# Performance work log

Measured on AMD Instinct MI355X. Metric: run time of the kernel, lower is better.

## Reference

```python
import jax, jax.numpy as jnp
import numpy as np

EPS = 1e-8
ITERS = 4
NEG = -1e9

def build_grid(H, W):
    y = jnp.linspace(-1.0, 1.0, H)
    x = jnp.linspace(-1.0, 1.0, W)
    yy, xx = jnp.meshgrid(y, x, indexing='ij')
    return jnp.stack([xx, yy], axis=-1)[None]  # (1,H,W,2)

def ln(x, g, b):
    m = jnp.mean(x, -1, keepdims=True)
    v = jnp.mean(jnp.square(x - m), -1, keepdims=True)
    return (x - m) * jax.lax.rsqrt(v + 1e-5) * g + b

def gru(x, h, wih, whh, bih, bhh):
    gi = x @ wih.T + bih
    gh = h @ whh.T + bhh
    ir, iz, inn = jnp.split(gi, 3, -1)
    hr, hz, hn = jnp.split(gh, 3, -1)
    r = jax.nn.sigmoid(ir + hr)
    z = jax.nn.sigmoid(iz + hz)
    n = jnp.tanh(inn + r * hn)
    return (1.0 - z) * n + z * h


def setup_inputs():
    B, H, W, C, D, K = 4, 128, 128, 64, 64, 4
    keys = iter(jax.random.split(jax.random.key(0), 64))
    def nrm(shape, s):
        return jax.random.normal(next(keys), shape, jnp.float32) * s
    sw = C ** -0.5
    sd = D ** -0.5
    inp = dict(
        feat=nrm((B, H, W, C), 1.0),
        mask=jax.random.randint(next(keys), (K, 1, H, W), 0, 2).astype(jnp.float32),
        noise_fg=nrm((B, K, D), 1.0),
        noise_bg=nrm((B, 1, D), 1.0),
        slots_mu=nrm((1, 1, D), 1.0),
        slots_logsigma=nrm((1, 1, D), 0.1),
        slots_mu_bg=nrm((1, 1, D), 1.0),
        slots_logsigma_bg=nrm((1, 1, D), 0.1),
        norm_feat_g=jnp.ones((C,)), norm_feat_b=jnp.zeros((C,)),
        grid_embed_w=nrm((C, 4), 0.5), grid_embed_b=jnp.zeros((C,)),
        k_fg_w=nrm((C, C), sw), v_fg_w=nrm((C, C), sw),
        k_bg_w=nrm((C, C), sw), v_bg_w=nrm((C, C), sw),
        mlp_fg_ln_g=jnp.ones((C,)), mlp_fg_ln_b=jnp.zeros((C,)),
        mlp_fg_w=nrm((D, C), sw), mlp_fg_b=jnp.zeros((D,)),
        mlp_bg_ln_g=jnp.ones((C,)), mlp_bg_ln_b=jnp.zeros((C,)),
        mlp_bg_w=nrm((D, C), sw), mlp_bg_b=jnp.zeros((D,)),
        q_ln_g=jnp.ones((D,)), q_ln_b=jnp.zeros((D,)), q_w=nrm((D, D), sd),
        qbg_ln_g=jnp.ones((D,)), qbg_ln_b=jnp.zeros((D,)), qbg_w=nrm((D, D), sd),
        gru_fg_wih=nrm((3 * D, D), sd), gru_fg_whh=nrm((3 * D, D), sd),
        gru_fg_bih=jnp.zeros((3 * D,)), gru_fg_bhh=jnp.zeros((3 * D,)),
        gru_bg_wih=nrm((3 * D, D), sd), gru_bg_whh=nrm((3 * D, D), sd),
        gru_bg_bih=jnp.zeros((3 * D,)), gru_bg_bhh=jnp.zeros((3 * D,)),
        res_fg_ln_g=jnp.ones((D,)), res_fg_ln_b=jnp.zeros((D,)),
        res_fg_w=nrm((D, D), sd), res_fg_b=jnp.zeros((D,)),
        res_bg_ln_g=jnp.ones((D,)), res_bg_ln_b=jnp.zeros((D,)),
        res_bg_w=nrm((D, D), sd), res_bg_b=jnp.zeros((D,)),
    )
    return inp


def reference(feat, mask, noise_fg, noise_bg, slots_mu, slots_logsigma,
              slots_mu_bg, slots_logsigma_bg, norm_feat_g, norm_feat_b,
              grid_embed_w, grid_embed_b, k_fg_w, v_fg_w, k_bg_w, v_bg_w,
              mlp_fg_ln_g, mlp_fg_ln_b, mlp_fg_w, mlp_fg_b,
              mlp_bg_ln_g, mlp_bg_ln_b, mlp_bg_w, mlp_bg_b,
              q_ln_g, q_ln_b, q_w, qbg_ln_g, qbg_ln_b, qbg_w,
              gru_fg_wih, gru_fg_whh, gru_fg_bih, gru_fg_bhh,
              gru_bg_wih, gru_bg_whh, gru_bg_bih, gru_bg_bhh,
              res_fg_ln_g, res_fg_ln_b, res_fg_w, res_fg_b,
              res_bg_ln_g, res_bg_ln_b, res_bg_w, res_bg_b):
    B, H, W, C = feat.shape
    N = H * W
    K = mask.shape[0]
    D = slots_mu.shape[-1]
    scale = D ** -0.5
    grid = build_grid(H, W)            # (1,H,W,2)
    grid_flat = grid.reshape(N, 2)
    feat = feat.reshape(B, N, C)
    # slot init (noise passed in for determinism)
    slot_fg = slots_mu + jnp.exp(slots_logsigma) * noise_fg       # (B,K,D)
    slot_bg = slots_mu_bg + jnp.exp(slots_logsigma_bg) * noise_bg  # (B,1,D)
    # fg positions = mask-weighted grid mean
    gk = jnp.transpose(grid[0], (2, 0, 1))[None]  # (1,2,H,W)
    fg_pos = (gk * mask).sum((2, 3)) / (mask.sum((1, 2, 3))[:, None] + 1e-5)  # (K,2)
    fg_pos = jnp.broadcast_to(fg_pos[None], (B, K, 2))
    feat = ln(feat, norm_feat_g, norm_feat_b)
    # background k,v (position-independent, computed once)
    rel_bg = jnp.concatenate([grid, -grid], -1).reshape(1, 1, N, 4)
    ge_bg = rel_bg @ grid_embed_w.T + grid_embed_b                # (1,1,N,C)
    kb = (feat @ k_bg_w.T)[:, None] + ge_bg                       # (B,1,N,C)
    vb = (feat @ v_bg_w.T)[:, None] + ge_bg
    k_bg = ln(kb, mlp_bg_ln_g, mlp_bg_ln_b) @ mlp_bg_w.T + mlp_bg_b
    v_bg = ln(vb, mlp_bg_ln_g, mlp_bg_ln_b) @ mlp_bg_w.T + mlp_bg_b
    mask_flat = mask.reshape(K, N)
    kf = feat @ k_fg_w.T   # iteration-invariant input projections
    vf = feat @ v_fg_w.T
    for _ in range(ITERS):
        prev_fg, prev_bg = slot_fg, slot_bg
        q_fg = ln(slot_fg, q_ln_g, q_ln_b) @ q_w.T
        q_bg = ln(slot_bg, qbg_ln_g, qbg_ln_b) @ qbg_w.T
        # position-relative grid embedding -> per-slot k,v
        rel = grid[:, None] - fg_pos[:, :, None, None, :]          # (B,K,H,W,2)
        rel = jnp.concatenate([rel, -rel], -1).reshape(B, K, N, 4)
        ge = rel @ grid_embed_w.T + grid_embed_b                   # (B,K,N,C)
        k = ln(kf[:, None] + ge, mlp_fg_ln_g, mlp_fg_ln_b) @ mlp_fg_w.T + mlp_fg_b
        v = ln(vf[:, None] + ge, mlp_fg_ln_g, mlp_fg_ln_b) @ mlp_fg_w.T + mlp_fg_b
        # background update
        attn_bg = jax.nn.softmax(jnp.einsum('bd,bnd->bn', q_bg[:, 0], k_bg[:, 0]) * scale, axis=1) + EPS
        upd_bg = jnp.einsum('bn,bnd->bd', attn_bg, v_bg[:, 0])
        sbg = gru(upd_bg, slot_bg[:, 0], gru_bg_wih, gru_bg_whh, gru_bg_bih, gru_bg_bhh)[:, None]
        slot_bg = ln(sbg, res_bg_ln_g, res_bg_ln_b) @ res_bg_w.T + res_bg_b + prev_bg
        # foreground update (vectorized over K slots)
        logits = jnp.einsum('bkd,bknd->bkn', q_fg, k) * scale
        logits = jnp.where(mask_flat[None] == 0, NEG, logits)
        attn = jax.nn.softmax(logits, axis=-1)
        upd_fg = jnp.einsum('bkn,bknd->bkd', attn, v)
        fg_pos = jnp.einsum('bkn,nd->bkd', attn, grid_flat)
        sfg = gru(upd_fg.reshape(-1, D), slot_fg.reshape(-1, D),
                  gru_fg_wih, gru_fg_whh, gru_fg_bih, gru_fg_bhh).reshape(B, K, D)
        slot_fg = ln(sfg, res_fg_ln_g, res_fg_ln_b) @ res_fg_w.T + res_fg_b + prev_fg
    slots = jnp.concatenate([slot_bg, slot_fg], axis=1)  # (B,K+1,D)
    return slots, fg_pos
```

## Files before the change

### kernel.cpp

```cpp
#include <hip/hip_runtime.h>
#include <math.h>

#define DEVI __device__ __forceinline__

constexpr int Bb = 4, Nn = 16384, Kk = 4;
constexpr int NCH = 64;
constexpr int CH = 256;
constexpr int FG_BLK = Bb * NCH;
constexpr int NBG = 64;
constexpr int BG_BLK = Bb * NBG;
constexpr int FG_PS = 72;
constexpr int BG_PS = 130;

typedef __attribute__((ext_vector_type(8))) short bf16x8;
typedef __attribute__((ext_vector_type(8))) unsigned short u16x8;
typedef __attribute__((ext_vector_type(4))) unsigned short u16x4;
typedef __attribute__((ext_vector_type(4))) float f32x4;

DEVI float bf2f(unsigned short u){ unsigned int x = ((unsigned int)u) << 16; return __builtin_bit_cast(float, x); }
DEVI unsigned short f2bf(float f){
  unsigned int u = __builtin_bit_cast(unsigned int, f);
  u += 0x7fffu + ((u >> 16) & 1u);
  return (unsigned short)(u >> 16);
}
DEVI float rsum_16_32(float v){ v += __shfl_xor(v,16); v += __shfl_xor(v,32); return v; }
DEVI float rmax_16_32(float v){ v = fmaxf(v,__shfl_xor(v,16)); v = fmaxf(v,__shfl_xor(v,32)); return v; }
DEVI float rsum_1_8(float v){ v += __shfl_xor(v,1); v += __shfl_xor(v,2); v += __shfl_xor(v,4); v += __shfl_xor(v,8); return v; }
DEVI float rmax_1_8(float v){ v = fmaxf(v,__shfl_xor(v,1)); v = fmaxf(v,__shfl_xor(v,2)); v = fmaxf(v,__shfl_xor(v,4)); v = fmaxf(v,__shfl_xor(v,8)); return v; }
DEVI float rsum_all(float v){ return rsum_16_32(rsum_1_8(v)); }
DEVI float rmax_all(float v){ return rmax_16_32(rmax_1_8(v)); }
DEVI float sel4(float a0, float a1, float a2, float a3, int r){
  float v = a0; v = (r == 1) ? a1 : v; v = (r == 2) ? a2 : v; v = (r == 3) ? a3 : v; return v;
}
DEVI float sigm(float x){ return 1.f / (1.f + __expf(-x)); }

constexpr float GSTEP = 2.0f / 127.0f;
DEVI float gxf(int n){ return (float)(n & 127) * GSTEP - 1.0f; }
DEVI float gyf(int n){ return (float)((n >> 7) & 127) * GSTEP - 1.0f; }

#define NEGINF (-__builtin_inff())

__global__ __launch_bounds__(1024) void k_setup(
    const float* __restrict__ mask,
    const float* __restrict__ gw, const float* __restrict__ gb,
    const float* __restrict__ g_fg, const float* __restrict__ bln_fg,
    const float* __restrict__ w_fg, const float* __restrict__ b_fg,
    float* __restrict__ fg_pos, float* __restrict__ cbuf)
{
  int t = threadIdx.x;
  if (blockIdx.x < 4) {
    int k = blockIdx.x;
    const float4* mp = (const float4*)(mask + (size_t)k * Nn);
    float sm = 0, sx = 0, sy = 0;
    #pragma unroll
    for (int i = 0; i < 4; ++i) {
      int idx = t + i * 1024;
      float4 v = mp[idx];
      int n = idx * 4;
      float gy = gyf(n);
      float rowsum = v.x + v.y + v.z + v.w;
      sm += rowsum;
      sx += v.x * gxf(n) + v.y * gxf(n + 1) + v.z * gxf(n + 2) + v.w * gxf(n + 3);
      sy += rowsum * gy;
    }
    sm = rsum_all(sm); sx = rsum_all(sx); sy = rsum_all(sy);
    __shared__ float red[3][16];
    int wv = t >> 6, l = t & 63;
    if (l == 0) { red[0][wv] = sm; red[1][wv] = sx; red[2][wv] = sy; }
    __syncthreads();
    if (t == 0) {
      float S = 0, X = 0, Y = 0;
      #pragma unroll
      for (int i = 0; i < 16; ++i) { S += red[0][i]; X += red[1][i]; Y += red[2][i]; }
      float inv = 1.f / (S + 1e-5f);
      float px = X * inv, py = Y * inv;
      for (int b = 0; b < 4; ++b) { fg_pos[(b*4+k)*2+0] = px; fg_pos[(b*4+k)*2+1] = py; }
    }
  } else {
    if (t < 64) {
      float gx_t = gw[t*4+0] - gw[t*4+2];
      float gy_t = gw[t*4+1] - gw[t*4+3];
      float aGx = 0, aGy = 0, agW = 0, aC0 = 0;
      for (int c = 0; c < 64; ++c) {
        float wv = w_fg[t*64 + c];
        float gc = g_fg[c];
        float gxc = gw[c*4+0] - gw[c*4+2];
        float gyc = gw[c*4+1] - gw[c*4+3];
        aGx += gxc * gc * wv;
        aGy += gyc * gc * wv;
        agW += gc * wv;
        aC0 += bln_fg[c] * wv;
      }
      cbuf[t] = aGx; cbuf[64+t] = aGy; cbuf[128+t] = agW; cbuf[192+t] = aC0 + b_fg[t];
      float mgx = rsum_all(gx_t) * (1.f/64.f);
      float mgy = rsum_all(gy_t) * (1.f/64.f);
      float egx2 = rsum_all(gx_t*gx_t) * (1.f/64.f);
      float egy2 = rsum_all(gy_t*gy_t) * (1.f/64.f);
      float egxy = rsum_all(gx_t*gy_t) * (1.f/64.f);
      if (t == 0) { cbuf[256]=mgx; cbuf[257]=mgy; cbuf[258]=egx2; cbuf[259]=egy2; cbuf[260]=egxy; }
    }
  }
}

__global__ __launch_bounds__(256) void k_prep(
    const float* __restrict__ feat,
    const float* __restrict__ norm_g, const float* __restrict__ norm_b,
    const float* __restrict__ gw, const float* __restrict__ gb,
    const float* __restrict__ k_fg_w, const float* __restrict__ v_fg_w,
    const float* __restrict__ k_bg_w, const float* __restrict__ v_bg_w,
    const float* __restrict__ mlp_bg_ln_g, const float* __restrict__ mlp_bg_ln_b,
    const float* __restrict__ mlp_bg_w, const float* __restrict__ mlp_bg_b,
    const float* __restrict__ mlp_fg_ln_g, const float* __restrict__ mlp_fg_w,
    unsigned short* __restrict__ A_k, unsigned short* __restrict__ A_vT,
    float* __restrict__ statsKV,
    unsigned short* __restrict__ kbg, unsigned short* __restrict__ vbg,
    const float* __restrict__ noise_fg, const float* __restrict__ noise_bg,
    const float* __restrict__ mu, const float* __restrict__ ls,
    const float* __restrict__ mub, const float* __restrict__ lsb,
    const float* __restrict__ q_ln_g, const float* __restrict__ q_ln_b, const float* __restrict__ q_w,
    const float* __restrict__ qbg_ln_g, const float* __restrict__ qbg_ln_b, const float* __restrict__ qbg_w,
    const float* __restrict__ cbuf,
    float* slot_fg, float* slot_bg, float* q_fg, float* q_bg, float* qscal)
{
  int tid = threadIdx.x, wave = tid >> 6, l = tid & 63;
  if ((int)blockIdx.x >= 512) {
    __shared__ float lds[64];
    int ib = blockIdx.x - 512;
    float lnv = 0.f;
    if (tid < 64) {
      if (ib < 16) {
        float s = mu[tid] + expf(ls[tid]) * noise_fg[ib * 64 + tid];
        slot_fg[ib * 64 + tid] = s;
        float mean = rsum_all(s) * (1.f / 64.f);
        float d = s - mean;
        float var = rsum_all(d * d) * (1.f / 64.f);
        lnv = d * rsqrtf(var + 1e-5f) * q_ln_g[tid] + q_ln_b[tid];
      } else {
        int b = ib - 16;
        float s = mub[tid] + expf(lsb[tid]) * noise_bg[b * 64 + tid];
        slot_bg[b * 64 + tid] = s;
        float mean = rsum_all(s) * (1.f / 64.f);
        float d = s - mean;
        float var = rsum_all(d * d) * (1.f / 64.f);
        lnv = d * rsqrtf(var + 1e-5f) * qbg_ln_g[tid] + qbg_ln_b[tid];
      }
      lds[tid] = lnv;
    }
    __syncthreads();
    if (tid < 64) {
      if (ib < 16) {
        float acc = 0.f;
        #pragma unroll 8
        for (int c = 0; c < 64; ++c) acc += q_w[tid * 64 + c] * lds[c];
        q_fg[ib * 64 + tid] = acc;
        float qGx = rsum_all(acc * cbuf[tid]);
        float qGy = rsum_all(acc * cbuf[64 + tid]);
        float qgW = rsum_all(acc * cbuf[128 + tid]);
        float qC0 = rsum_all(acc * cbuf[192 + tid]);
        if (tid == 0) { qscal[ib*4+0]=qGx; qscal[ib*4+1]=qGy; qscal[ib*4+2]=qgW; qscal[ib*4+3]=qC0; }
      } else {
        int b = ib - 16;
        float acc = 0.f;
        #pragma unroll 8
        for (int c = 0; c < 64; ++c) acc += qbg_w[tid * 64 + c] * lds[c];
        q_bg[b * 64 + tid] = acc;
      }
    }
    return;
  }
  __shared__ bf16x8 wfrag[6 * 8 * 64];
  __shared__ __align__(16) unsigned short tbuf[4][16][88];
  __shared__ float s_gwx[64], s_gwy[64], s_gb[64], s_mlg[64], s_mlb[64], s_mbb[64], s_gf[64];
  const float* wsrc[6] = { k_fg_w, v_fg_w, k_bg_w, v_bg_w, mlp_bg_w, mlp_fg_w };
  for (int mi = wave; mi < 6; mi += 4) {
    const float* ws = wsrc[mi];
    #pragma unroll
    for (int f = 0; f < 8; ++f) {
      int ct = f >> 1, kh = f & 1;
      int row = ct * 16 + (l & 15);
      int c0 = ((l >> 4) << 3) + kh * 32;
      bf16x8 v;
      #pragma unroll
      for (int j = 0; j < 8; ++j) v[j] = (short)f2bf(ws[row * 64 + c0 + j]);
      wfrag[(mi * 8 + f) * 64 + l] = v;
    }
  }
  if (tid < 64) {
    s_gwx[tid] = gw[tid*4+0] - gw[tid*4+2];
    s_gwy[tid] = gw[tid*4+1] - gw[tid*4+3];
    s_gb[tid]  = gb[tid];
    s_mlg[tid] = mlp_bg_ln_g[tid];
    s_mlb[tid] = mlp_bg_ln_b[tid];
    s_mbb[tid] = mlp_bg_b[tid];
    s_gf[tid]  = mlp_fg_ln_g[tid];
  }
  __syncthreads();

  int cb = (l >> 4) << 3;
  float ngr[16], nbr[16];
  #pragma unroll
  for (int j = 0; j < 16; ++j) {
    int col = (j < 8) ? (cb + j) : (32 + cb + j - 8);
    ngr[j] = norm_g[col]; nbr[j] = norm_b[col];
  }
  float gwxD[4], gwyD[4], gbD[4], mlgD[4], mlbD[4], mbbD[4], gfD[4];
  #pragma unroll
  for (int ct = 0; ct < 4; ++ct) {
    int col = ct * 16 + (l & 15);
    gwxD[ct] = s_gwx[col]; gwyD[ct] = s_gwy[col]; gbD[ct] = s_gb[col];
    mlgD[ct] = s_mlg[col]; mlbD[ct] = s_mlb[col]; mbbD[ct] = s_mbb[col];
    gfD[ct] = s_gf[col];
  }

  int wg = blockIdx.x * 4 + wave;
  for (int tt = 0; tt < 2; ++tt) {
    int tile = wg * 2 + tt;
    int rowg = tile * 16 + (l & 15);
    const float* fp = feat + (size_t)rowg * 64;
    float x[16];
    #pragma unroll
    for (int j = 0; j < 8; ++j) x[j] = fp[cb + j];
    #pragma unroll
    for (int j = 0; j < 8; ++j) x[8 + j] = fp[32 + cb + j];
    float sm = 0;
    #pragma unroll
    for (int j = 0; j < 16; ++j) sm += x[j];
    float mean = rsum_16_32(sm) * (1.f / 64.f);
    float vv = 0;
    #pragma unroll
    for (int j = 0; j < 16; ++j) { float d = x[j] - mean; vv += d * d; }
    float rstd = rsqrtf(rsum_16_32(vv) * (1.f / 64.f) + 1e-5f);
    bf16x8 a0, a1;
    #pragma unroll
    for (int j = 0; j < 8; ++j) a0[j] = (short)f2bf((x[j] - mean) * rstd * ngr[j] + nbr[j]);
    #pragma unroll
    for (int j = 0; j < 8; ++j) a1[j] = (short)f2bf((x[8 + j] - mean) * rstd * ngr[8 + j] + nbr[8 + j]);

    for (int mi = 0; mi < 4; ++mi) {
      f32x4 acc[4];
      #pragma unroll
      for (int ct = 0; ct < 4; ++ct) acc[ct] = (f32x4){0.f, 0.f, 0.f, 0.f};
      #pragma unroll
      for (int ct = 0; ct < 4; ++ct) {
        acc[ct] = __builtin_amdgcn_mfma_f32_16x16x32_bf16(a0, wfrag[(mi * 8 + ct * 2 + 0) * 64 + l], acc[ct], 0, 0, 0);
        acc[ct] = __builtin_amdgcn_mfma_f32_16x16x32_bf16(a1, wfrag[(mi * 8 + ct * 2 + 1) * 64 + l], acc[ct], 0, 0, 0);
      }
      if (mi < 2) {
        #pragma unroll
        for (int ct = 0; ct < 4; ++ct)
          #pragma unroll
          for (int r = 0; r < 4; ++r)
            acc[ct][r] += gbD[ct];
        float s1[4], s2[4], sx[4], sy[4];
        #pragma unroll
        for (int r = 0; r < 4; ++r) {
          float a0v = acc[0][r], a1v = acc[1][r], a2v = acc[2][r], a3v = acc[3][r];
          s1[r] = rsum_1_8(a0v + a1v + a2v + a3v);
          s2[r] = rsum_1_8(a0v*a0v + a1v*a1v + a2v*a2v + a3v*a3v);
          sx[r] = rsum_1_8(a0v*gwxD[0] + a1v*gwxD[1] + a2v*gwxD[2] + a3v*gwxD[3]);
          sy[r] = rsum_1_8(a0v*gwyD[0] + a1v*gwyD[1] + a2v*gwyD[2] + a3v*gwyD[3]);
        }
        int rsel = l & 15;
        if (rsel < 4) {
          float4 stv;
          stv.x = sel4(s1[0], s1[1], s1[2], s1[3], rsel) * (1.f/64.f);
          stv.y = sel4(s2[0], s2[1], s2[2], s2[3], rsel) * (1.f/64.f);
          stv.z = sel4(sx[0], sx[1], sx[2], sx[3], rsel) * (1.f/64.f);
          stv.w = sel4(sy[0], sy[1], sy[2], sy[3], rsel) * (1.f/64.f);
          int frow = tile * 16 + (l >> 4) * 4 + rsel;
          *(float4*)(statsKV + (size_t)frow * 8 + mi * 4) = stv;
        }
        #pragma unroll
        for (int ct = 0; ct < 4; ++ct)
          #pragma unroll
          for (int r = 0; r < 4; ++r)
            tbuf[wave][(l >> 4) * 4 + r][ct * 16 + (l & 15)] = f2bf(acc[ct][r] * gfD[ct]);
        bf16x8 b0 = *(const bf16x8*)&tbuf[wave][l & 15][cb];
        bf16x8 b1 = *(const bf16x8*)&tbuf[wave][l & 15][32 + cb];
        f32x4 acc2[4];
        #pragma unroll
        for (int ct = 0; ct < 4; ++ct) acc2[ct] = (f32x4){0.f, 0.f, 0.f, 0.f};
        #pragma unroll
        for (int ct = 0; ct < 4; ++ct) {
          acc2[ct] = __builtin_amdgcn_mfma_f32_16x16x32_bf16(b0, wfrag[(5 * 8 + ct * 2 + 0) * 64 + l], acc2[ct], 0, 0, 0);
          acc2[ct] = __builtin_amdgcn_mfma_f32_16x16x32_bf16(b1, wfrag[(5 * 8 + ct * 2 + 1) * 64 + l], acc2[ct], 0, 0, 0);
        }
        if (mi == 0) {
          #pragma unroll
          for (int ct = 0; ct < 4; ++ct)
            #pragma unroll
            for (int r = 0; r < 4; ++r)
              tbuf[wave][(l >> 4) * 4 + r][ct * 16 + (l & 15)] = f2bf(acc2[ct][r]);
          u16x8 o0 = *(const u16x8*)&tbuf[wave][l & 15][cb];
          u16x8 o1 = *(const u16x8*)&tbuf[wave][l & 15][32 + cb];
          *(u16x8*)(A_k + (size_t)rowg * 64 + cb) = o0;
          *(u16x8*)(A_k + (size_t)rowg * 64 + 32 + cb) = o1;
        } else {
          int bb = tile >> 10;
          int nb4 = (tile * 16 + ((l >> 4) << 2)) & (Nn - 1);
          #pragma unroll
          for (int ct = 0; ct < 4; ++ct) {
            u16x4 u4;
            u4[0] = f2bf(acc2[ct][0]); u4[1] = f2bf(acc2[ct][1]);
            u4[2] = f2bf(acc2[ct][2]); u4[3] = f2bf(acc2[ct][3]);
            int d = ct * 16 + (l & 15);
            *(u16x4*)(A_vT + ((size_t)bb * 64 + d) * Nn + nb4) = u4;
          }
        }
      } else {
        #pragma unroll
        for (int ct = 0; ct < 4; ++ct)
          #pragma unroll
          for (int r = 0; r < 4; ++r) {
            int n = (tile * 16 + (l >> 4) * 4 + r) & (Nn - 1);
            acc[ct][r] += gwxD[ct] * gxf(n) + gwyD[ct] * gyf(n) + gbD[ct];
          }
        float mrow[4], rstd2[4];
        #pragma unroll
        for (int r = 0; r < 4; ++r) {
          float srow = acc[0][r] + acc[1][r] + acc[2][r] + acc[3][r];
          srow = rsum_1_8(srow);
          mrow[r] = srow * (1.f / 64.f);
          float vr = 0;
          #pragma unroll
          for (int ct = 0; ct < 4; ++ct) { float d = acc[ct][r] - mrow[r]; vr += d * d; }
          vr = rsum_1_8(vr);
          rstd2[r] = rsqrtf(vr * (1.f / 64.f) + 1e-5f);
        }
        #pragma unroll
        for (int ct = 0; ct < 4; ++ct)
          #pragma unroll
          for (int r = 0; r < 4; ++r)
            tbuf[wave][(l >> 4) * 4 + r][ct * 16 + (l & 15)] =
                f2bf((acc[ct][r] - mrow[r]) * rstd2[r] * mlgD[ct] + mlbD[ct]);
        bf16x8 b0 = *(const bf16x8*)&tbuf[wave][l & 15][cb];
        bf16x8 b1 = *(const bf16x8*)&tbuf[wave][l & 15][32 + cb];
        f32x4 acc2[4];
        #pragma unroll
        for (int ct = 0; ct < 4; ++ct) acc2[ct] = (f32x4){0.f, 0.f, 0.f, 0.f};
        #pragma unroll
        for (int ct = 0; ct < 4; ++ct) {
          acc2[ct] = __builtin_amdgcn_mfma_f32_16x16x32_bf16(b0, wfrag[(4 * 8 + ct * 2 + 0) * 64 + l], acc2[ct], 0, 0, 0);
          acc2[ct] = __builtin_amdgcn_mfma_f32_16x16x32_bf16(b1, wfrag[(4 * 8 + ct * 2 + 1) * 64 + l], acc2[ct], 0, 0, 0);
        }
        #pragma unroll
        for (int ct = 0; ct < 4; ++ct)
          #pragma unroll
          for (int r = 0; r < 4; ++r)
            tbuf[wave][(l >> 4) * 4 + r][ct * 16 + (l & 15)] = f2bf(acc2[ct][r] + mbbD[ct]);
        unsigned short* dst = (mi == 2) ? kbg : vbg;
        u16x8 o0 = *(const u16x8*)&tbuf[wave][l & 15][cb];
        u16x8 o1 = *(const u16x8*)&tbuf[wave][l & 15][32 + cb];
        *(u16x8*)(dst + (size_t)rowg * 64 + cb) = o0;
        *(u16x8*)(dst + (size_t)rowg * 64 + 32 + cb) = o1;
      }
    }
  }
}

__global__ __launch_bounds__(256) void k_iter(
    const unsigned short* __restrict__ A_k, const unsigned short* __restrict__ A_vT,
    const float* __restrict__ statsKV,
    const unsigned short* __restrict__ kbg, const unsigned short* __restrict__ vbg,
    const float* __restrict__ q_fg, const float* __restrict__ q_bg,
    const float* __restrict__ fg_pos, const float* __restrict__ mask,
    const float* __restrict__ cbuf, const float* __restrict__ qscal,
    float* __restrict__ fgP, float* __restrict__ bgP)
{
  __shared__ float qa_pl[4][260];
  __shared__ __align__(16) unsigned short w_buf[4][272];
  __shared__ float redv[4][4][64];
  __shared__ float shred[4][130];
  int tid = threadIdx.x, wave = tid >> 6, l = tid & 63;
  if ((int)blockIdx.x < FG_BLK) {
    int b = blockIdx.x >> 6, ch = blockIdx.x & 63;
    int n0 = ch * CH;
    int slot = l & 15;
    bf16x8 qf0, qf1;
    {
      int bkq = b * 4 + (slot & 3);
      #pragma unroll
      for (int j = 0; j < 8; ++j) {
        float v0 = q_fg[bkq * 64 + (l >> 4) * 8 + j];
        float v1 = q_fg[bkq * 64 + 32 + (l >> 4) * 8 + j];
        qf0[j] = (short)f2bf(slot < 4 ? v0 : 0.f);
        qf1[j] = (short)f2bf(slot < 4 ? v1 : 0.f);
      }
    }
    #pragma unroll
    for (int tt2 = 0; tt2 < 4; ++tt2) {
      int t = wave * 4 + tt2;
      const unsigned short* ap = A_k + ((size_t)b * Nn + n0 + t * 16 + (l & 15)) * 64 + ((l >> 4) << 3);
      bf16x8 b0 = *(const bf16x8*)ap;
      bf16x8 b1 = *(const bf16x8*)(ap + 32);
      f32x4 acc = (f32x4){0.f, 0.f, 0.f, 0.f};
      acc = __builtin_amdgcn_mfma_f32_16x16x32_bf16(qf0, b0, acc, 0, 0, 0);
      acc = __builtin_amdgcn_mfma_f32_16x16x32_bf16(qf1, b1, acc, 0, 0, 0);
      if (l < 16) {
        #pragma unroll
        for (int r = 0; r < 4; ++r) qa_pl[r][t * 16 + l] = acc[r];
      }
    }
    __syncthreads();
    int w = wave;
    float pxw = fg_pos[(b * 4 + w) * 2 + 0], pyw = fg_pos[(b * 4 + w) * 2 + 1];
    float qGx = qscal[(b*4+w)*4+0], qGy = qscal[(b*4+w)*4+1];
    float qgW = qscal[(b*4+w)*4+2], qC0 = qscal[(b*4+w)*4+3];
    float mgx = cbuf[256], mgy = cbuf[257], egx2 = cbuf[258], egy2 = cbuf[259], egxy = cbuf[260];
    float lgc[4], rsv[4], muvc[4];
    float mx = NEGINF;
    #pragma unroll
    for (int i = 0; i < 4; ++i) {
      int n = n0 + i * 64 + l;
      const float* st = statsKV + ((size_t)b * Nn + n) * 8;
      float4 sk = *(const float4*)st;
      float4 sv = *(const float4*)(st + 4);
      float gx = gxf(n), gy = gyf(n);
      float relx = gx - pxw, rely = gy - pyw;
      float mu = sk.x + relx * mgx + rely * mgy;
      float ex2 = sk.y + 2.f*(relx*sk.z + rely*sk.w) + relx*relx*egx2 + rely*rely*egy2 + 2.f*relx*rely*egxy;
      float rstd = rsqrtf(fmaxf(ex2 - mu * mu, 0.f) + 1e-5f);
      float qa = qa_pl[w][i * 64 + l];
      float lg = 0.125f * (rstd * (qa + relx * qGx + rely * qGy - mu * qgW) + qC0);
      float mk = mask[w * Nn + n];
      lg = (mk == 0.f) ? -1e9f : lg;
      lgc[i] = lg; mx = fmaxf(mx, lg);
      float muv = sv.x + relx * mgx + rely * mgy;
      float ex2v = sv.y + 2.f*(relx*sv.z + rely*sv.w) + relx*relx*egx2 + rely*rely*egy2 + 2.f*relx*rely*egxy;
      rsv[i] = rsqrtf(fmaxf(ex2v - muv * muv, 0.f) + 1e-5f);
      muvc[i] = muv;
    }
    float mb = rmax_all(mx);
    float s_a = 0, px_a = 0, py_a = 0, swx = 0, swy = 0, swm = 0;
    #pragma unroll
    for (int i = 0; i < 4; ++i) {
      int n = n0 + i * 64 + l;
      float e = __expf(lgc[i] - mb);
      float gx = gxf(n), gy = gyf(n);
      s_a += e; px_a += e * gx; py_a += e * gy;
      float wgt = e * rsv[i];
      swx += wgt * (gx - pxw); swy += wgt * (gy - pyw); swm += wgt * muvc[i];
      w_buf[w][i * 64 + l] = f2bf(wgt);
    }
    s_a = rsum_all(s_a); px_a = rsum_all(px_a); py_a = rsum_all(py_a);
    swx = rsum_all(swx); swy = rsum_all(swy); swm = rsum_all(swm);
    if (l == 0) {
      float* P = fgP + ((size_t)(b * NCH + ch) * 4 + w) * FG_PS;
      P[0] = mb; P[1] = s_a; P[2] = px_a; P[3] = py_a; P[4] = swx; P[5] = swy; P[6] = swm;
    }
    __syncthreads();
    f32x4 acc[4];
    #pragma unroll
    for (int ct = 0; ct < 4; ++ct) acc[ct] = (f32x4){0.f, 0.f, 0.f, 0.f};
    bf16x8 zz;
    #pragma unroll
    for (int j = 0; j < 8; ++j) zz[j] = 0;
    #pragma unroll
    for (int st2 = 0; st2 < 2; ++st2) {
      int noff = wave * 64 + st2 * 32;
      bf16x8 wf = *(const bf16x8*)&w_buf[l & 3][noff + ((l >> 4) << 3)];
      if ((l & 15) >= 4) wf = zz;
      #pragma unroll
      for (int ct = 0; ct < 4; ++ct) {
        const unsigned short* ap = A_vT + ((size_t)b * 64 + ct * 16 + (l & 15)) * Nn + n0 + noff + ((l >> 4) << 3);
        bf16x8 bv = *(const bf16x8*)ap;
        acc[ct] = __builtin_amdgcn_mfma_f32_16x16x32_bf16(wf, bv, acc[ct], 0, 0, 0);
      }
    }
    if (l < 16) {
      #pragma unroll
      for (int ct = 0; ct < 4; ++ct)
        #pragma unroll
        for (int r = 0; r < 4; ++r)
          redv[wave][r][ct * 16 + l] = acc[ct][r];
    }
    __syncthreads();
    if (wave == 0) {
      #pragma unroll
      for (int s2 = 0; s2 < 4; ++s2) {
        float v = redv[0][s2][l] + redv[1][s2][l] + redv[2][s2][l] + redv[3][s2][l];
        fgP[((size_t)(b * NCH + ch) * 4 + s2) * FG_PS + 8 + l] = v;
      }
    }
  } else {
    int idx = blockIdx.x - FG_BLK;
    int b = idx >> 6, nb = idx & 63;
    int cb16 = (l >> 4) << 4;
    float qr[16];
    #pragma unroll
    for (int i = 0; i < 16; ++i) qr[i] = q_bg[b * 64 + cb16 + i];
    float m = NEGINF, s = 0.f, upd[16], sv[16];
    #pragma unroll
    for (int i = 0; i < 16; ++i) { upd[i] = 0; sv[i] = 0; }
    #pragma unroll
    for (int pass = 0; pass < 4; ++pass) {
      int nrow = nb * 256 + pass * 64 + wave * 16 + (l & 15);
      const unsigned short* kp = kbg + ((size_t)b * Nn + nrow) * 64 + cb16;
      const unsigned short* vp = vbg + ((size_t)b * Nn + nrow) * 64 + cb16;
      u16x8 k0 = *(const u16x8*)kp, k1 = *(const u16x8*)(kp + 8);
      u16x8 v0 = *(const u16x8*)vp, v1 = *(const u16x8*)(vp + 8);
      float p = 0;
      #pragma unroll
      for (int i = 0; i < 8; ++i) { p += qr[i] * bf2f(k0[i]); p += qr[8 + i] * bf2f(k1[i]); }
      p = rsum_16_32(p);
      float lg = 0.125f * p;
      float tm = rmax_1_8(lg);
      float mnew = fmaxf(m, tm);
      float alpha = __expf(m - mnew); m = mnew;
      s *= alpha;
      #pragma unroll
      for (int i = 0; i < 16; ++i) upd[i] *= alpha;
      float e = __expf(lg - mnew);
      s += e;
      #pragma unroll
      for (int i = 0; i < 8; ++i) {
        float fv0 = bf2f(v0[i]), fv1 = bf2f(v1[i]);
        upd[i] += e * fv0; upd[8 + i] += e * fv1;
        sv[i] += fv0; sv[8 + i] += fv1;
      }
    }
    s = rsum_1_8(s);
    #pragma unroll
    for (int i = 0; i < 16; ++i) { upd[i] = rsum_1_8(upd[i]); sv[i] = rsum_1_8(sv[i]); }
    if (l == 0) { shred[wave][0] = m; shred[wave][1] = s; }
    if ((l & 15) == 0) {
      int g = l >> 4;
      #pragma unroll
      for (int i = 0; i < 16; ++i) { shred[wave][2 + g * 16 + i] = upd[i]; shred[wave][66 + g * 16 + i] = sv[i]; }
    }
    __syncthreads();
    if (wave == 0) {
      float m0 = shred[0][0], m1 = shred[1][0], m2 = shred[2][0], m3 = shred[3][0];
      float mg = fmaxf(fmaxf(m0, m1), fmaxf(m2, m3));
      float w0 = __expf(m0 - mg), w1 = __expf(m1 - mg), w2 = __expf(m2 - mg), w3 = __expf(m3 - mg);
      float* P = bgP + (size_t)idx * BG_PS;
      P[2 + l]  = w0 * shred[0][2 + l] + w1 * shred[1][2 + l] + w2 * shred[2][2 + l] + w3 * shred[3][2 + l];
      P[66 + l] = shred[0][66 + l] + shred[1][66 + l] + shred[2][66 + l] + shred[3][66 + l];
      if (l == 0) {
        P[0] = mg;
        P[1] = w0 * shred[0][1] + w1 * shred[1][1] + w2 * shred[2][1] + w3 * shred[3][1];
      }
    }
  }
}

__global__ __launch_bounds__(256) void k_comb(
    const float* __restrict__ fgP, const float* __restrict__ bgP,
    float* slot_fg, float* slot_bg,
    float* q_fg, float* q_bg, float* fg_pos, float* qscal,
    const float* __restrict__ cbuf,
    const float* __restrict__ gru_fg_wih, const float* __restrict__ gru_fg_whh,
    const float* __restrict__ gru_fg_bih, const float* __restrict__ gru_fg_bhh,
    const float* __restrict__ gru_bg_wih, const float* __restrict__ gru_bg_whh,
    const float* __restrict__ gru_bg_bih, const float* __restrict__ gru_bg_bhh,
    const float* __restrict__ res_fg_ln_g, const float* __restrict__ res_fg_ln_b,
    const float* __restrict__ res_fg_w, const float* __restrict__ res_fg_b,
    const float* __restrict__ res_bg_ln_g, const float* __restrict__ res_bg_ln_b,
    const float* __restrict__ res_bg_w, const float* __restrict__ res_bg_b,
    const float* __restrict__ q_ln_g, const float* __restrict__ q_ln_b, const float* __restrict__ q_w,
    const float* __restrict__ qbg_ln_g, const float* __restrict__ qbg_ln_b, const float* __restrict__ qbg_w,
    float* __restrict__ dout)
{
  __shared__ float wl[64];
  __shared__ float ubuf[4][64];
  __shared__ float part[4][64];
  __shared__ float xs[64], hs[64];
  __shared__ float gd[384];
  __shared__ float scal[6];
  int tid = threadIdx.x, wv = tid >> 6, l = tid & 63;
  int blk = blockIdx.x;
  if (blk < 16) {
    int bk = blk, b = bk >> 2, k = bk & 3;
    if (wv == 0) {
      const float* pp = fgP + ((size_t)(b * NCH + l) * 4 + k) * FG_PS;
      float mp = pp[0];
      float sp = pp[1];
      float pxp = pp[2];
      float pyp = pp[3];
      float sxp = pp[4];
      float syp = pp[5];
      float smp = pp[6];
      float mg = rmax_all(mp);
      float w = __expf(mp - mg);
      wl[l] = w;
      float S = rsum_all(w * sp);
      float px = rsum_all(w * pxp);
      float py = rsum_all(w * pyp);
      float sxg = rsum_all(w * sxp);
      float syg = rsum_all(w * syp);
      float smg = rsum_all(w * smp);
      if (l == 0) { scal[0]=S; scal[1]=px/S; scal[2]=py/S; scal[3]=sxg; scal[4]=syg; scal[5]=smg; }
    }
    __syncthreads();
    float S = scal[0];
    float acc = 0;
    #pragma unroll
    for (int i = 0; i < 16; ++i) {
      int c = wv * 16 + i;
      acc += wl[c] * fgP[((size_t)(b * NCH + c) * 4 + k) * FG_PS + 8 + l];
    }
    ubuf[wv][l] = acc;
    __syncthreads();
    if (wv == 0) {
      float UV = ubuf[0][l] + ubuf[1][l] + ubuf[2][l] + ubuf[3][l];
      float upd = (UV + scal[3] * cbuf[l] + scal[4] * cbuf[64 + l] - scal[5] * cbuf[128 + l]) / S + cbuf[192 + l];
      xs[l] = upd;
      hs[l] = slot_fg[bk * 64 + l];
    }
    __syncthreads();
    {
      int r = tid;
      float a;
      if (r < 192) {
        const float* w = gru_fg_wih + r * 64; a = gru_fg_bih[r];
        #pragma unroll 8
        for (int c = 0; c < 64; ++c) a += w[c] * xs[c];
      } else {
        const float* w = gru_fg_whh + (r - 192) * 64; a = gru_fg_bhh[r - 192];
        #pragma unroll 8
        for (int c = 0; c < 64; ++c) a += w[c] * hs[c];
      }
      gd[r] = a;
      if (tid < 128) {
        int r2 = tid + 256;
        const float* w = gru_fg_whh + (r2 - 192) * 64; float a2 = gru_fg_bhh[r2 - 192];
        #pragma unroll 8
        for (int c = 0; c < 64; ++c) a2 += w[c] * hs[c];
        gd[r2] = a2;
      }
    }
    __syncthreads();
    if (wv == 0) {
      float h = hs[l];
      float r = sigm(gd[l] + gd[192 + l]);
      float z = sigm(gd[64 + l] + gd[256 + l]);
      float nng = tanhf(gd[128 + l] + r * gd[320 + l]);
      float hnew = (1.f - z) * nng + z * h;
      float mean = rsum_all(hnew) * (1.f / 64.f);
      float d = hnew - mean;
      float var = rsum_all(d * d) * (1.f / 64.f);
      xs[l] = d * rsqrtf(var + 1e-5f) * res_fg_ln_g[l] + res_fg_ln_b[l];
    }
    __syncthreads();
    {
      int c0 = wv * 16;
      const float* w = res_fg_w + l * 64 + c0;
      float a = 0;
      #pragma unroll
      for (int c = 0; c < 16; ++c) a += w[c] * xs[c0 + c];
      part[wv][l] = a;
    }
    __syncthreads();
    if (wv == 0) {
      float h = hs[l];
      float snew = part[0][l] + part[1][l] + part[2][l] + part[3][l] + res_fg_b[l] + h;
      slot_fg[bk * 64 + l] = snew;
      dout[(b * 5 + 1 + k) * 64 + l] = snew;
      float mq = rsum_all(snew) * (1.f / 64.f);
      float dq = snew - mq;
      float vq = rsum_all(dq * dq) * (1.f / 64.f);
      xs[l] = dq * rsqrtf(vq + 1e-5f) * q_ln_g[l] + q_ln_b[l];
    }
    __syncthreads();
    {
      int c0 = wv * 16;
      const float* w = q_w + l * 64 + c0;
      float a = 0;
      #pragma unroll
      for (int c = 0; c < 16; ++c) a += w[c] * xs[c0 + c];
      part[wv][l] = a;
    }
    __syncthreads();
    if (wv == 0) {
      float qacc = part[0][l] + part[1][l] + part[2][l] + part[3][l];
      q_fg[bk * 64 + l] = qacc;
      float qGx = rsum_all(qacc * cbuf[l]);
      float qGy = rsum_all(qacc * cbuf[64 + l]);
      float qgW = rsum_all(qacc * cbuf[128 + l]);
      float qC0 = rsum_all(qacc * cbuf[192 + l]);
      if (l == 0) {
        qscal[bk*4+0]=qGx; qscal[bk*4+1]=qGy; qscal[bk*4+2]=qgW; qscal[bk*4+3]=qC0;
        float px = scal[1], py = scal[2];
        fg_pos[bk * 2 + 0] = px; fg_pos[bk * 2 + 1] = py;
        dout[1280 + bk * 2 + 0] = px; dout[1280 + bk * 2 + 1] = py;
      }
    }
  } else {
    int b = blk - 16;
    const float* P = bgP + (size_t)b * NBG * BG_PS;
    if (wv == 0) {
      float mp = P[l * BG_PS + 0];
      float sp = P[l * BG_PS + 1];
      float mg = rmax_all(mp);
      float w = __expf(mp - mg);
      wl[l] = w;
      float S = rsum_all(w * sp);
      if (l == 0) scal[0] = S;
    }
    __syncthreads();
    float S = scal[0];
    float acc = 0, sva = 0;
    #pragma unroll
    for (int i = 0; i < 16; ++i) {
      int p = wv * 16 + i;
      acc += wl[p] * P[(size_t)p * BG_PS + 2 + l];
      sva += P[(size_t)p * BG_PS + 66 + l];
    }
    ubuf[wv][l] = acc; part[wv][l] = sva;
    __syncthreads();
    if (wv == 0) {
      float upd = (ubuf[0][l] + ubuf[1][l] + ubuf[2][l] + ubuf[3][l]) / S
                + 1e-8f * (part[0][l] + part[1][l] + part[2][l] + part[3][l]);
      xs[l] = upd;
      hs[l] = slot_bg[b * 64 + l];
    }
    __syncthreads();
    {
      int r = tid;
      float a;
      if (r < 192) {
        const float* w = gru_bg_wih + r * 64; a = gru_bg_bih[r];
        #pragma unroll 8
        for (int c = 0; c < 64; ++c) a += w[c] * xs[c];
      } else {
        const float* w = gru_bg_whh + (r - 192) * 64; a = gru_bg_bhh[r - 192];
        #pragma unroll 8
        for (int c = 0; c < 64; ++c) a += w[c] * hs[c];
      }
      gd[r] = a;
      if (tid < 128) {
        int r2 = tid + 256;
        const float* w = gru_bg_whh + (r2 - 192) * 64; float a2 = gru_bg_bhh[r2 - 192];
        #pragma unroll 8
        for (int c = 0; c < 64; ++c) a2 += w[c] * hs[c];
        gd[r2] = a2;
      }
    }
    __syncthreads();
    if (wv == 0) {
      float h = hs[l];
      float r = sigm(gd[l] + gd[192 + l]);
      float z = sigm(gd[64 + l] + gd[256 + l]);
      float nng = tanhf(gd[128 + l] + r * gd[320 + l]);
      float hnew = (1.f - z) * nng + z * h;
      float mean = rsum_all(hnew) * (1.f / 64.f);
      float d = hnew - mean;
      float var = rsum_all(d * d) * (1.f / 64.f);
      xs[l] = d * rsqrtf(var + 1e-5f) * res_bg_ln_g[l] + res_bg_ln_b[l];
    }
    __syncthreads();
    {
      int c0 = wv * 16;
      const float* w = res_bg_w + l * 64 + c0;
      float a = 0;
      #pragma unroll
      for (int c = 0; c < 16; ++c) a += w[c] * xs[c0 + c];
      part[wv][l] = a;
    }
    __syncthreads();
    if (wv == 0) {
      float h = hs[l];
      float snew = part[0][l] + part[1][l] + part[2][l] + part[3][l] + res_bg_b[l] + h;
      slot_bg[b * 64 + l] = snew;
      dout[(b * 5 + 0) * 64 + l] = snew;
      float mq = rsum_all(snew) * (1.f / 64.f);
      float dq = snew - mq;
      float vq = rsum_all(dq * dq) * (1.f / 64.f);
      xs[l] = dq * rsqrtf(vq + 1e-5f) * qbg_ln_g[l] + qbg_ln_b[l];
    }
    __syncthreads();
    {
      int c0 = wv * 16;
      const float* w = qbg_w + l * 64 + c0;
      float a = 0;
      #pragma unroll
      for (int c = 0; c < 16; ++c) a += w[c] * xs[c0 + c];
      part[wv][l] = a;
    }
    __syncthreads();
    if (wv == 0) {
      q_bg[b * 64 + l] = part[0][l] + part[1][l] + part[2][l] + part[3][l];
    }
  }
}

extern "C" void kernel_launch(void* const* d_in, const int* in_sizes, int n_in,
                              void* d_out, int out_size, void* d_ws, size_t ws_size,
                              hipStream_t stream)
{
  (void)in_sizes; (void)n_in; (void)out_size; (void)ws_size;
  const float* feat        = (const float*)d_in[0];
  const float* mask        = (const float*)d_in[1];
  const float* noise_fg    = (const float*)d_in[2];
  const float* noise_bg    = (const float*)d_in[3];
  const float* slots_mu    = (const float*)d_in[4];
  const float* slots_ls    = (const float*)d_in[5];
  const float* slots_mu_bg = (const float*)d_in[6];
  const float* slots_ls_bg = (const float*)d_in[7];
  const float* norm_feat_g = (const float*)d_in[8];
  const float* norm_feat_b = (const float*)d_in[9];
  const float* grid_embed_w= (const float*)d_in[10];
  const float* grid_embed_b= (const float*)d_in[11];
  const float* k_fg_w      = (const float*)d_in[12];
  const float* v_fg_w      = (const float*)d_in[13];
  const float* k_bg_w      = (const float*)d_in[14];
  const float* v_bg_w      = (const float*)d_in[15];
  const float* mlp_fg_ln_g = (const float*)d_in[16];
  const float* mlp_fg_ln_b = (const float*)d_in[17];
  const float* mlp_fg_w    = (const float*)d_in[18];
  const float* mlp_fg_b    = (const float*)d_in[19];
  const float* mlp_bg_ln_g = (const float*)d_in[20];
  const float* mlp_bg_ln_b = (const float*)d_in[21];
  const float* mlp_bg_w    = (const float*)d_in[22];
  const float* mlp_bg_b    = (const float*)d_in[23];
  const float* q_ln_g      = (const float*)d_in[24];
  const float* q_ln_b      = (const float*)d_in[25];
  const float* q_w         = (const float*)d_in[26];
  const float* qbg_ln_g    = (const float*)d_in[27];
  const float* qbg_ln_b    = (const float*)d_in[28];
  const float* qbg_w       = (const float*)d_in[29];
  const float* gru_fg_wih  = (const float*)d_in[30];
  const float* gru_fg_whh  = (const float*)d_in[31];
  const float* gru_fg_bih  = (const float*)d_in[32];
  const float* gru_fg_bhh  = (const float*)d_in[33];
  const float* gru_bg_wih  = (const float*)d_in[34];
  const float* gru_bg_whh  = (const float*)d_in[35];
  const float* gru_bg_bih  = (const float*)d_in[36];
  const float* gru_bg_bhh  = (const float*)d_in[37];
  const float* res_fg_ln_g = (const float*)d_in[38];
  const float* res_fg_ln_b = (const float*)d_in[39];
  const float* res_fg_w    = (const float*)d_in[40];
  const float* res_fg_b    = (const float*)d_in[41];
  const float* res_bg_ln_g = (const float*)d_in[42];
  const float* res_bg_ln_b = (const float*)d_in[43];
  const float* res_bg_w    = (const float*)d_in[44];
  const float* res_bg_b    = (const float*)d_in[45];
  float* dout = (float*)d_out;

  char* wsp = (char*)d_ws;
  size_t off = 0;
  auto alloc = [&](size_t bytes) -> void* {
    void* p = wsp + off;
    off += (bytes + 255) & ~(size_t)255;
    return p;
  };
  unsigned short* A_k  = (unsigned short*)alloc((size_t)Bb * Nn * 64 * 2);
  unsigned short* A_vT = (unsigned short*)alloc((size_t)Bb * Nn * 64 * 2);
  float* statsKV       = (float*)alloc((size_t)Bb * Nn * 8 * 4);
  unsigned short* kbg  = (unsigned short*)alloc((size_t)Bb * Nn * 64 * 2);
  unsigned short* vbg  = (unsigned short*)alloc((size_t)Bb * Nn * 64 * 2);
  float* slot_fg = (float*)alloc(16 * 64 * 4);
  float* slot_bg = (float*)alloc(4 * 64 * 4);
  float* q_fg    = (float*)alloc(16 * 64 * 4);
  float* q_bg    = (float*)alloc(4 * 64 * 4);
  float* fg_pos  = (float*)alloc(16 * 2 * 4);
  float* qscal   = (float*)alloc(16 * 4 * 4);
  float* cbuf    = (float*)alloc(264 * 4);
  float* fgP     = (float*)alloc((size_t)Bb * NCH * 4 * FG_PS * 4);
  float* bgP     = (float*)alloc((size_t)BG_BLK * BG_PS * 4);

  k_setup<<<5, 1024, 0, stream>>>(mask, grid_embed_w, grid_embed_b, mlp_fg_ln_g, mlp_fg_ln_b,
                                  mlp_fg_w, mlp_fg_b, fg_pos, cbuf);
  k_prep<<<532, 256, 0, stream>>>(feat, norm_feat_g, norm_feat_b, grid_embed_w, grid_embed_b,
                                  k_fg_w, v_fg_w, k_bg_w, v_bg_w,
                                  mlp_bg_ln_g, mlp_bg_ln_b, mlp_bg_w, mlp_bg_b,
                                  mlp_fg_ln_g, mlp_fg_w,
                                  A_k, A_vT, statsKV, kbg, vbg,
                                  noise_fg, noise_bg, slots_mu, slots_ls, slots_mu_bg, slots_ls_bg,
                                  q_ln_g, q_ln_b, q_w, qbg_ln_g, qbg_ln_b, qbg_w, cbuf,
                                  slot_fg, slot_bg, q_fg, q_bg, qscal);
  for (int it = 0; it < 4; ++it) {
    k_iter<<<FG_BLK + BG_BLK, 256, 0, stream>>>(A_k, A_vT, statsKV, kbg, vbg,
                                                q_fg, q_bg, fg_pos, mask, cbuf, qscal,
                                                fgP, bgP);
    k_comb<<<20, 256, 0, stream>>>(fgP, bgP, slot_fg, slot_bg, q_fg, q_bg, fg_pos, qscal, cbuf,
                                   gru_fg_wih, gru_fg_whh, gru_fg_bih, gru_fg_bhh,
                                   gru_bg_wih, gru_bg_whh, gru_bg_bih, gru_bg_bhh,
                                   res_fg_ln_g, res_fg_ln_b, res_fg_w, res_fg_b,
                                   res_bg_ln_g, res_bg_ln_b, res_bg_w, res_bg_b,
                                   q_ln_g, q_ln_b, q_w, qbg_ln_g, qbg_ln_b, qbg_w,
                                   dout);
  }
}
```

Before: 116.8 us.

## Fuse slot update into iteration kernel with ping-pong buffers, merge setup into prep

Removes the per-iteration combine kernel: each k_iter block redundantly recomputes the previous iteration's reduction, GRU, residual MLP and query projection from double-buffered partials before doing its attention pass. k_setup is folded into k_prep as extra blocks, and k_prep now processes one tile per wave with twice as many blocks. A final k_fin kernel produces the outputs. This cuts kernel launches and serialization gaps but adds redundant per-block GRU/MLP work and extra global reads of the partial buffers.

```diff
diff --git a/kernel.cpp b/kernel.cpp
--- a/kernel.cpp
+++ b/kernel.cpp
@@ -40,68 +40,6 @@
 
 #define NEGINF (-__builtin_inff())
 
-__global__ __launch_bounds__(1024) void k_setup(
-    const float* __restrict__ mask,
-    const float* __restrict__ gw, const float* __restrict__ gb,
-    const float* __restrict__ g_fg, const float* __restrict__ bln_fg,
-    const float* __restrict__ w_fg, const float* __restrict__ b_fg,
-    float* __restrict__ fg_pos, float* __restrict__ cbuf)
-{
-  int t = threadIdx.x;
-  if (blockIdx.x < 4) {
-    int k = blockIdx.x;
-    const float4* mp = (const float4*)(mask + (size_t)k * Nn);
-    float sm = 0, sx = 0, sy = 0;
-    #pragma unroll
-    for (int i = 0; i < 4; ++i) {
-      int idx = t + i * 1024;
-      float4 v = mp[idx];
-      int n = idx * 4;
-      float gy = gyf(n);
-      float rowsum = v.x + v.y + v.z + v.w;
-      sm += rowsum;
-      sx += v.x * gxf(n) + v.y * gxf(n + 1) + v.z * gxf(n + 2) + v.w * gxf(n + 3);
-      sy += rowsum * gy;
-    }
-    sm = rsum_all(sm); sx = rsum_all(sx); sy = rsum_all(sy);
-    __shared__ float red[3][16];
-    int wv = t >> 6, l = t & 63;
-    if (l == 0) { red[0][wv] = sm; red[1][wv] = sx; red[2][wv] = sy; }
-    __syncthreads();
-    if (t == 0) {
-      float S = 0, X = 0, Y = 0;
-      #pragma unroll
-      for (int i = 0; i < 16; ++i) { S += red[0][i]; X += red[1][i]; Y += red[2][i]; }
-      float inv = 1.f / (S + 1e-5f);
-      float px = X * inv, py = Y * inv;
-      for (int b = 0; b < 4; ++b) { fg_pos[(b*4+k)*2+0] = px; fg_pos[(b*4+k)*2+1] = py; }
-    }
-  } else {
-    if (t < 64) {
-      float gx_t = gw[t*4+0] - gw[t*4+2];
-      float gy_t = gw[t*4+1] - gw[t*4+3];
-      float aGx = 0, aGy = 0, agW = 0, aC0 = 0;
-      for (int c = 0; c < 64; ++c) {
-        float wv = w_fg[t*64 + c];
-        float gc = g_fg[c];
-        float gxc = gw[c*4+0] - gw[c*4+2];
-        float gyc = gw[c*4+1] - gw[c*4+3];
-        aGx += gxc * gc * wv;
-        aGy += gyc * gc * wv;
-        agW += gc * wv;
-        aC0 += bln_fg[c] * wv;
-      }
-      cbuf[t] = aGx; cbuf[64+t] = aGy; cbuf[128+t] = agW; cbuf[192+t] = aC0 + b_fg[t];
-      float mgx = rsum_all(gx_t) * (1.f/64.f);
-      float mgy = rsum_all(gy_t) * (1.f/64.f);
-      float egx2 = rsum_all(gx_t*gx_t) * (1.f/64.f);
-      float egy2 = rsum_all(gy_t*gy_t) * (1.f/64.f);
-      float egxy = rsum_all(gx_t*gy_t) * (1.f/64.f);
-      if (t == 0) { cbuf[256]=mgx; cbuf[257]=mgy; cbuf[258]=egx2; cbuf[259]=egy2; cbuf[260]=egxy; }
-    }
-  }
-}
-
 __global__ __launch_bounds__(256) void k_prep(
     const float* __restrict__ feat,
     const float* __restrict__ norm_g, const float* __restrict__ norm_b,
@@ -110,7 +48,9 @@
     const float* __restrict__ k_bg_w, const float* __restrict__ v_bg_w,
     const float* __restrict__ mlp_bg_ln_g, const float* __restrict__ mlp_bg_ln_b,
     const float* __restrict__ mlp_bg_w, const float* __restrict__ mlp_bg_b,
-    const float* __restrict__ mlp_fg_ln_g, const float* __restrict__ mlp_fg_w,
+    const float* __restrict__ mlp_fg_ln_g, const float* __restrict__ mlp_fg_ln_b,
+    const float* __restrict__ mlp_fg_w, const float* __restrict__ mlp_fg_b,
+    const float* __restrict__ mask,
     unsigned short* __restrict__ A_k, unsigned short* __restrict__ A_vT,
     float* __restrict__ statsKV,
     unsigned short* __restrict__ kbg, unsigned short* __restrict__ vbg,
@@ -119,51 +59,100 @@
     const float* __restrict__ mub, const float* __restrict__ lsb,
     const float* __restrict__ q_ln_g, const float* __restrict__ q_ln_b, const float* __restrict__ q_w,
     const float* __restrict__ qbg_ln_g, const float* __restrict__ qbg_ln_b, const float* __restrict__ qbg_w,
-    const float* __restrict__ cbuf,
-    float* slot_fg, float* slot_bg, float* q_fg, float* q_bg, float* qscal)
+    float* slot_fg0, float* slot_bg0, float* q_fg, float* q_bg,
+    float* __restrict__ fg_pos, float* __restrict__ cbuf)
 {
   int tid = threadIdx.x, wave = tid >> 6, l = tid & 63;
-  if ((int)blockIdx.x >= 512) {
-    __shared__ float lds[64];
-    int ib = blockIdx.x - 512;
-    float lnv = 0.f;
-    if (tid < 64) {
-      if (ib < 16) {
-        float s = mu[tid] + expf(ls[tid]) * noise_fg[ib * 64 + tid];
-        slot_fg[ib * 64 + tid] = s;
-        float mean = rsum_all(s) * (1.f / 64.f);
-        float d = s - mean;
-        float var = rsum_all(d * d) * (1.f / 64.f);
-        lnv = d * rsqrtf(var + 1e-5f) * q_ln_g[tid] + q_ln_b[tid];
-      } else {
-        int b = ib - 16;
-        float s = mub[tid] + expf(lsb[tid]) * noise_bg[b * 64 + tid];
-        slot_bg[b * 64 + tid] = s;
-        float mean = rsum_all(s) * (1.f / 64.f);
-        float d = s - mean;
-        float var = rsum_all(d * d) * (1.f / 64.f);
-        lnv = d * rsqrtf(var + 1e-5f) * qbg_ln_g[tid] + qbg_ln_b[tid];
-      }
-      lds[tid] = lnv;
-    }
-    __syncthreads();
-    if (tid < 64) {
-      if (ib < 16) {
-        float acc = 0.f;
-        #pragma unroll 8
-        for (int c = 0; c < 64; ++c) acc += q_w[tid * 64 + c] * lds[c];
-        q_fg[ib * 64 + tid] = acc;
-        float qGx = rsum_all(acc * cbuf[tid]);
-        float qGy = rsum_all(acc * cbuf[64 + tid]);
-        float qgW = rsum_all(acc * cbuf[128 + tid]);
-        float qC0 = rsum_all(acc * cbuf[192 + tid]);
-        if (tid == 0) { qscal[ib*4+0]=qGx; qscal[ib*4+1]=qGy; qscal[ib*4+2]=qgW; qscal[ib*4+3]=qC0; }
-      } else {
-        int b = ib - 16;
-        float acc = 0.f;
-        #pragma unroll 8
-        for (int c = 0; c < 64; ++c) acc += qbg_w[tid * 64 + c] * lds[c];
-        q_bg[b * 64 + tid] = acc;
+  if ((int)blockIdx.x >= 1024) {
+    int ib = blockIdx.x - 1024;
+    if (ib < 4) {
+      int k = ib;
+      const float4* mp = (const float4*)(mask + (size_t)k * Nn);
+      float sm = 0, sx = 0, sy = 0;
+      #pragma unroll
+      for (int i = 0; i < 16; ++i) {
+        int idx = tid + i * 256;
+        float4 v = mp[idx];
+        int n = idx * 4;
+        float gy = gyf(n);
+        float rowsum = v.x + v.y + v.z + v.w;
+        sm += rowsum;
+        sx += v.x * gxf(n) + v.y * gxf(n + 1) + v.z * gxf(n + 2) + v.w * gxf(n + 3);
+        sy += rowsum * gy;
+      }
+      sm = rsum_all(sm); sx = rsum_all(sx); sy = rsum_all(sy);
+      __shared__ float red[3][4];
+      if (l == 0) { red[0][wave] = sm; red[1][wave] = sx; red[2][wave] = sy; }
+      __syncthreads();
+      if (tid == 0) {
+        float S = red[0][0]+red[0][1]+red[0][2]+red[0][3];
+        float X = red[1][0]+red[1][1]+red[1][2]+red[1][3];
+        float Y = red[2][0]+red[2][1]+red[2][2]+red[2][3];
+        float inv = 1.f / (S + 1e-5f);
+        float px = X * inv, py = Y * inv;
+        for (int b = 0; b < 4; ++b) { fg_pos[(b*4+k)*2+0] = px; fg_pos[(b*4+k)*2+1] = py; }
+      }
+    } else if (ib == 4) {
+      if (tid < 64) {
+        int t = tid;
+        float gx_t = gw[t*4+0] - gw[t*4+2];
+        float gy_t = gw[t*4+1] - gw[t*4+3];
+        float aGx = 0, aGy = 0, agW = 0, aC0 = 0;
+        for (int c = 0; c < 64; ++c) {
+          float wv = mlp_fg_w[t*64 + c];
+          float gc = mlp_fg_ln_g[c];
+          float gxc = gw[c*4+0] - gw[c*4+2];
+          float gyc = gw[c*4+1] - gw[c*4+3];
+          aGx += gxc * gc * wv;
+          aGy += gyc * gc * wv;
+          agW += gc * wv;
+          aC0 += mlp_fg_ln_b[c] * wv;
+        }
+        cbuf[t] = aGx; cbuf[64+t] = aGy; cbuf[128+t] = agW; cbuf[192+t] = aC0 + mlp_fg_b[t];
+        float mgx = rsum_all(gx_t) * (1.f/64.f);
+        float mgy = rsum_all(gy_t) * (1.f/64.f);
+        float egx2 = rsum_all(gx_t*gx_t) * (1.f/64.f);
+        float egy2 = rsum_all(gy_t*gy_t) * (1.f/64.f);
+        float egxy = rsum_all(gx_t*gy_t) * (1.f/64.f);
+        if (t == 0) { cbuf[256]=mgx; cbuf[257]=mgy; cbuf[258]=egx2; cbuf[259]=egy2; cbuf[260]=egxy; }
+      }
+    } else {
+      __shared__ float lds[64];
+      int jb = ib - 5;
+      if (tid < 64) {
+        float lnv;
+        if (jb < 16) {
+          float s = mu[tid] + expf(ls[tid]) * noise_fg[jb * 64 + tid];
+          slot_fg0[jb * 64 + tid] = s;
+          float mean = rsum_all(s) * (1.f / 64.f);
+          float d = s - mean;
+          float var = rsum_all(d * d) * (1.f / 64.f);
+          lnv = d * rsqrtf(var + 1e-5f) * q_ln_g[tid] + q_ln_b[tid];
+        } else {
+          int b = jb - 16;
+          float s = mub[tid] + expf(lsb[tid]) * noise_bg[b * 64 + tid];
+          slot_bg0[b * 64 + tid] = s;
+          float mean = rsum_all(s) * (1.f / 64.f);
+          float d = s - mean;
+          float var = rsum_all(d * d) * (1.f / 64.f);
+          lnv = d * rsqrtf(var + 1e-5f) * qbg_ln_g[tid] + qbg_ln_b[tid];
+        }
+        lds[tid] = lnv;
+      }
+      __syncthreads();
+      if (tid < 64) {
+        if (jb < 16) {
+          float acc = 0.f;
+          #pragma unroll 8
+          for (int c = 0; c < 64; ++c) acc += q_w[tid * 64 + c] * lds[c];
+          q_fg[jb * 64 + tid] = acc;
+        } else {
+          int b = jb - 16;
+          float acc = 0.f;
+          #pragma unroll 8
+          for (int c = 0; c < 64; ++c) acc += qbg_w[tid * 64 + c] * lds[c];
+          q_bg[b * 64 + tid] = acc;
+        }
       }
     }
     return;
@@ -212,9 +201,8 @@
     gfD[ct] = s_gf[col];
   }
 
-  int wg = blockIdx.x * 4 + wave;
-  for (int tt = 0; tt < 2; ++tt) {
-    int tile = wg * 2 + tt;
+  int tile = blockIdx.x * 4 + wave;
+  {
     int rowg = tile * 16 + (l & 15);
     const float* fp = feat + (size_t)rowg * 64;
     float x[16];
@@ -359,30 +347,124 @@
 }
 
 __global__ __launch_bounds__(256) void k_iter(
+    int it,
     const unsigned short* __restrict__ A_k, const unsigned short* __restrict__ A_vT,
     const float* __restrict__ statsKV,
     const unsigned short* __restrict__ kbg, const unsigned short* __restrict__ vbg,
-    const float* __restrict__ q_fg, const float* __restrict__ q_bg,
-    const float* __restrict__ fg_pos, const float* __restrict__ mask,
-    const float* __restrict__ cbuf, const float* __restrict__ qscal,
-    float* __restrict__ fgP, float* __restrict__ bgP)
+    const float* __restrict__ q_fg0, const float* __restrict__ q_bg0,
+    const float* __restrict__ fg_pos0, const float* __restrict__ mask,
+    const float* __restrict__ cbuf,
+    const float* __restrict__ fgP_r, float* __restrict__ fgP_w,
+    const float* __restrict__ bgP_r, float* __restrict__ bgP_w,
+    const float* __restrict__ slotfg_r, float* __restrict__ slotfg_w,
+    const float* __restrict__ slotbg_r, float* __restrict__ slotbg_w,
+    const float* __restrict__ gfg_wih, const float* __restrict__ gfg_whh,
+    const float* __restrict__ gfg_bih, const float* __restrict__ gfg_bhh,
+    const float* __restrict__ gbg_wih, const float* __restrict__ gbg_whh,
+    const float* __restrict__ gbg_bih, const float* __restrict__ gbg_bhh,
+    const float* __restrict__ rfg_g, const float* __restrict__ rfg_b2,
+    const float* __restrict__ rfg_w, const float* __restrict__ rfg_bb,
+    const float* __restrict__ rbg_g, const float* __restrict__ rbg_b2,
+    const float* __restrict__ rbg_w, const float* __restrict__ rbg_bb,
+    const float* __restrict__ qln_g, const float* __restrict__ qln_b, const float* __restrict__ qw,
+    const float* __restrict__ qbgln_g, const float* __restrict__ qbgln_b, const float* __restrict__ qbgw)
 {
   __shared__ float qa_pl[4][260];
   __shared__ __align__(16) unsigned short w_buf[4][272];
   __shared__ float redv[4][4][64];
   __shared__ float shred[4][130];
+  __shared__ float xsw[4][64], hsw[4][64];
+  __shared__ float qsh[4][64];
   int tid = threadIdx.x, wave = tid >> 6, l = tid & 63;
   if ((int)blockIdx.x < FG_BLK) {
     int b = blockIdx.x >> 6, ch = blockIdx.x & 63;
     int n0 = ch * CH;
+    int w = wave;
+    float px, py, qGx, qGy, qgW, qC0;
+    if (it == 0) {
+      float qv = q_fg0[(b * 4 + w) * 64 + l];
+      qsh[w][l] = qv;
+      qGx = rsum_all(qv * cbuf[l]);
+      qGy = rsum_all(qv * cbuf[64 + l]);
+      qgW = rsum_all(qv * cbuf[128 + l]);
+      qC0 = rsum_all(qv * cbuf[192 + l]);
+      px = fg_pos0[(b * 4 + w) * 2 + 0];
+      py = fg_pos0[(b * 4 + w) * 2 + 1];
+      __syncthreads();
+    } else {
+      const float* Pb = fgP_r + ((size_t)(b * 64 + l) * 4 + w) * FG_PS;
+      float mp = Pb[0], sp = Pb[1], pxp = Pb[2], pyp = Pb[3];
+      float sxp = Pb[4], syp = Pb[5], smp = Pb[6];
+      float mg = rmax_all(mp);
+      float wgt = __expf(mp - mg);
+      float S = rsum_all(wgt * sp);
+      px = rsum_all(wgt * pxp) / S;
+      py = rsum_all(wgt * pyp) / S;
+      float sxg = rsum_all(wgt * sxp);
+      float syg = rsum_all(wgt * syp);
+      float smg = rsum_all(wgt * smp);
+      float ua = 0;
+      #pragma unroll 8
+      for (int c = 0; c < 64; ++c) {
+        float wc = __shfl(wgt, c);
+        ua += wc * fgP_r[((size_t)(b * 64 + c) * 4 + w) * FG_PS + 8 + l];
+      }
+      float upd = (ua + sxg * cbuf[l] + syg * cbuf[64 + l] - smg * cbuf[128 + l]) / S + cbuf[192 + l];
+      float h = slotfg_r[(b * 4 + w) * 64 + l];
+      xsw[w][l] = upd; hsw[w][l] = h;
+      __syncthreads();
+      float gir = gfg_bih[l], giz = gfg_bih[64 + l], gin = gfg_bih[128 + l];
+      float ghr = gfg_bhh[l], ghz = gfg_bhh[64 + l], ghn = gfg_bhh[128 + l];
+      #pragma unroll 8
+      for (int c = 0; c < 64; ++c) {
+        float u = xsw[w][c], hh = hsw[w][c];
+        gir += gfg_wih[l * 64 + c] * u;
+        giz += gfg_wih[(64 + l) * 64 + c] * u;
+        gin += gfg_wih[(128 + l) * 64 + c] * u;
+        ghr += gfg_whh[l * 64 + c] * hh;
+        ghz += gfg_whh[(64 + l) * 64 + c] * hh;
+        ghn += gfg_whh[(128 + l) * 64 + c] * hh;
+      }
+      float r = sigm(gir + ghr), z = sigm(giz + ghz);
+      float nng = tanhf(gin + r * ghn);
+      float hnew = (1.f - z) * nng + z * h;
+      float mean = rsum_all(hnew) * (1.f / 64.f);
+      float d = hnew - mean;
+      float var = rsum_all(d * d) * (1.f / 64.f);
+      float lnv = d * rsqrtf(var + 1e-5f) * rfg_g[l] + rfg_b2[l];
+      __syncthreads();
+      xsw[w][l] = lnv;
+      __syncthreads();
+      float acc2 = 0;
+      #pragma unroll 8
+      for (int c = 0; c < 64; ++c) acc2 += rfg_w[l * 64 + c] * xsw[w][c];
+      float snew = acc2 + rfg_bb[l] + h;
+      if (ch == 0) slotfg_w[(b * 4 + w) * 64 + l] = snew;
+      float mq = rsum_all(snew) * (1.f / 64.f);
+      float dq = snew - mq;
+      float vq = rsum_all(dq * dq) * (1.f / 64.f);
+      float lnq = dq * rsqrtf(vq + 1e-5f) * qln_g[l] + qln_b[l];
+      __syncthreads();
+      xsw[w][l] = lnq;
+      __syncthreads();
+      float qacc = 0;
+      #pragma unroll 8
+      for (int c = 0; c < 64; ++c) qacc += qw[l * 64 + c] * xsw[w][c];
+      qsh[w][l] = qacc;
+      qGx = rsum_all(qacc * cbuf[l]);
+      qGy = rsum_all(qacc * cbuf[64 + l]);
+      qgW = rsum_all(qacc * cbuf[128 + l]);
+      qC0 = rsum_all(qacc * cbuf[192 + l]);
+      __syncthreads();
+    }
     int slot = l & 15;
     bf16x8 qf0, qf1;
     {
-      int bkq = b * 4 + (slot & 3);
+      int bkq = slot & 3;
       #pragma unroll
       for (int j = 0; j < 8; ++j) {
-        float v0 = q_fg[bkq * 64 + (l >> 4) * 8 + j];
-        float v1 = q_fg[bkq * 64 + 32 + (l >> 4) * 8 + j];
+        float v0 = qsh[bkq][(l >> 4) * 8 + j];
+        float v1 = qsh[bkq][32 + (l >> 4) * 8 + j];
         qf0[j] = (short)f2bf(slot < 4 ? v0 : 0.f);
         qf1[j] = (short)f2bf(slot < 4 ? v1 : 0.f);
       }
@@ -402,10 +484,6 @@
       }
     }
     __syncthreads();
-    int w = wave;
-    float pxw = fg_pos[(b * 4 + w) * 2 + 0], pyw = fg_pos[(b * 4 + w) * 2 + 1];
-    float qGx = qscal[(b*4+w)*4+0], qGy = qscal[(b*4+w)*4+1];
-    float qgW = qscal[(b*4+w)*4+2], qC0 = qscal[(b*4+w)*4+3];
     float mgx = cbuf[256], mgy = cbuf[257], egx2 = cbuf[258], egy2 = cbuf[259], egxy = cbuf[260];
     float lgc[4], rsv[4], muvc[4];
     float mx = NEGINF;
@@ -416,7 +494,7 @@
       float4 sk = *(const float4*)st;
       float4 sv = *(const float4*)(st + 4);
       float gx = gxf(n), gy = gyf(n);
-      float relx = gx - pxw, rely = gy - pyw;
+      float relx = gx - px, rely = gy - py;
       float mu = sk.x + relx * mgx + rely * mgy;
       float ex2 = sk.y + 2.f*(relx*sk.z + rely*sk.w) + relx*relx*egx2 + rely*rely*egy2 + 2.f*relx*rely*egxy;
       float rstd = rsqrtf(fmaxf(ex2 - mu * mu, 0.f) + 1e-5f);
@@ -438,14 +516,14 @@
       float e = __expf(lgc[i] - mb);
       float gx = gxf(n), gy = gyf(n);
       s_a += e; px_a += e * gx; py_a += e * gy;
-      float wgt = e * rsv[i];
-      swx += wgt * (gx - pxw); swy += wgt * (gy - pyw); swm += wgt * muvc[i];
-      w_buf[w][i * 64 + l] = f2bf(wgt);
+      float wgt2 = e * rsv[i];
+      swx += wgt2 * (gx - px); swy += wgt2 * (gy - py); swm += wgt2 * muvc[i];
+      w_buf[w][i * 64 + l] = f2bf(wgt2);
     }
     s_a = rsum_all(s_a); px_a = rsum_all(px_a); py_a = rsum_all(py_a);
     swx = rsum_all(swx); swy = rsum_all(swy); swm = rsum_all(swm);
     if (l == 0) {
-      float* P = fgP + ((size_t)(b * NCH + ch) * 4 + w) * FG_PS;
+      float* P = fgP_w + ((size_t)(b * NCH + ch) * 4 + w) * FG_PS;
       P[0] = mb; P[1] = s_a; P[2] = px_a; P[3] = py_a; P[4] = swx; P[5] = swy; P[6] = swm;
     }
     __syncthreads();
@@ -479,7 +557,7 @@
       #pragma unroll
       for (int s2 = 0; s2 < 4; ++s2) {
         float v = redv[0][s2][l] + redv[1][s2][l] + redv[2][s2][l] + redv[3][s2][l];
-        fgP[((size_t)(b * NCH + ch) * 4 + s2) * FG_PS + 8 + l] = v;
+        fgP_w[((size_t)(b * NCH + ch) * 4 + s2) * FG_PS + 8 + l] = v;
       }
     }
   } else {
@@ -487,8 +565,86 @@
     int b = idx >> 6, nb = idx & 63;
     int cb16 = (l >> 4) << 4;
     float qr[16];
-    #pragma unroll
-    for (int i = 0; i < 16; ++i) qr[i] = q_bg[b * 64 + cb16 + i];
+    if (it == 0) {
+      #pragma unroll
+      for (int i = 0; i < 16; ++i) qr[i] = q_bg0[b * 64 + cb16 + i];
+    } else {
+      __shared__ float wlb[64];
+      __shared__ float scS;
+      __shared__ float xsb[64], hsb2[64], qshbg[64];
+      if (wave == 0) {
+        const float* pbp = bgP_r + (size_t)(b * NBG + l) * BG_PS;
+        float mp = pbp[0], sp = pbp[1];
+        float mg = rmax_all(mp);
+        float wgt = __expf(mp - mg);
+        wlb[l] = wgt;
+        float S = rsum_all(wgt * sp);
+        if (l == 0) scS = S;
+      }
+      __syncthreads();
+      float acc = 0, sva = 0;
+      #pragma unroll
+      for (int i = 0; i < 16; ++i) {
+        int p = wave * 16 + i;
+        acc += wlb[p] * bgP_r[(size_t)(b * NBG + p) * BG_PS + 2 + l];
+        sva += bgP_r[(size_t)(b * NBG + p) * BG_PS + 66 + l];
+      }
+      shred[wave][l] = acc; shred[wave][66 + l] = sva;
+      __syncthreads();
+      if (wave == 0) {
+        float upd = (shred[0][l] + shred[1][l] + shred[2][l] + shred[3][l]) / scS
+                  + 1e-8f * (shred[0][66 + l] + shred[1][66 + l] + shred[2][66 + l] + shred[3][66 + l]);
+        float h = slotbg_r[b * 64 + l];
+        xsb[l] = upd; hsb2[l] = h;
+      }
+      __syncthreads();
+      if (wave == 0) {
+        float h = hsb2[l];
+        float gir = gbg_bih[l], giz = gbg_bih[64 + l], gin = gbg_bih[128 + l];
+        float ghr = gbg_bhh[l], ghz = gbg_bhh[64 + l], ghn = gbg_bhh[128 + l];
+        #pragma unroll 8
+        for (int c = 0; c < 64; ++c) {
+          float u = xsb[c], hh = hsb2[c];
+          gir += gbg_wih[l * 64 + c] * u;
+          giz += gbg_wih[(64 + l) * 64 + c] * u;
+          gin += gbg_wih[(128 + l) * 64 + c] * u;
+          ghr += gbg_whh[l * 64 + c] * hh;
+          ghz += gbg_whh[(64 + l) * 64 + c] * hh;
+          ghn += gbg_whh[(128 + l) * 64 + c] * hh;
+        }
+        float r = sigm(gir + ghr), z = sigm(giz + ghz);
+        float nng = tanhf(gin + r * ghn);
+        float hnew = (1.f - z) * nng + z * h;
+        float mean = rsum_all(hnew) * (1.f / 64.f);
+        float d = hnew - mean;
+        float var = rsum_all(d * d) * (1.f / 64.f);
+        xsb[l] = d * rsqrtf(var + 1e-5f) * rbg_g[l] + rbg_b2[l];
+      }
+      __syncthreads();
+      if (wave == 0) {
+        float h = hsb2[l];
+        float acc2 = 0;
+        #pragma unroll 8
+        for (int c = 0; c < 64; ++c) acc2 += rbg_w[l * 64 + c] * xsb[c];
+        float snew = acc2 + rbg_bb[l] + h;
+        if (nb == 0) slotbg_w[b * 64 + l] = snew;
+        float mq = rsum_all(snew) * (1.f / 64.f);
+        float dq = snew - mq;
+        float vq = rsum_all(dq * dq) * (1.f / 64.f);
+        hsb2[l] = dq * rsqrtf(vq + 1e-5f) * qbgln_g[l] + qbgln_b[l];
+      }
+      __syncthreads();
+      if (wave == 0) {
+        float qacc = 0;
+        #pragma unroll 8
+        for (int c = 0; c < 64; ++c) qacc += qbgw[l * 64 + c] * hsb2[c];
+        qshbg[l] = qacc;
+      }
+      __syncthreads();
+      #pragma unroll
+      for (int i = 0; i < 16; ++i) qr[i] = qshbg[cb16 + i];
+      __syncthreads();
+    }
     float m = NEGINF, s = 0.f, upd[16], sv[16];
     #pragma unroll
     for (int i = 0; i < 16; ++i) { upd[i] = 0; sv[i] = 0; }
@@ -533,7 +689,7 @@
       float m0 = shred[0][0], m1 = shred[1][0], m2 = shred[2][0], m3 = shred[3][0];
       float mg = fmaxf(fmaxf(m0, m1), fmaxf(m2, m3));
       float w0 = __expf(m0 - mg), w1 = __expf(m1 - mg), w2 = __expf(m2 - mg), w3 = __expf(m3 - mg);
-      float* P = bgP + (size_t)idx * BG_PS;
+      float* P = bgP_w + (size_t)idx * BG_PS;
       P[2 + l]  = w0 * shred[0][2 + l] + w1 * shred[1][2 + l] + w2 * shred[2][2 + l] + w3 * shred[3][2 + l];
       P[66 + l] = shred[0][66 + l] + shred[1][66 + l] + shred[2][66 + l] + shred[3][66 + l];
       if (l == 0) {
@@ -544,21 +700,18 @@
   }
 }
 
-__global__ __launch_bounds__(256) void k_comb(
+__global__ __launch_bounds__(256) void k_fin(
     const float* __restrict__ fgP, const float* __restrict__ bgP,
-    float* slot_fg, float* slot_bg,
-    float* q_fg, float* q_bg, float* fg_pos, float* qscal,
+    const float* __restrict__ slotfg, const float* __restrict__ slotbg,
     const float* __restrict__ cbuf,
-    const float* __restrict__ gru_fg_wih, const float* __restrict__ gru_fg_whh,
-    const float* __restrict__ gru_fg_bih, const float* __restrict__ gru_fg_bhh,
-    const float* __restrict__ gru_bg_wih, const float* __restrict__ gru_bg_whh,
-    const float* __restrict__ gru_bg_bih, const float* __restrict__ gru_bg_bhh,
-    const float* __restrict__ res_fg_ln_g, const float* __restrict__ res_fg_ln_b,
-    const float* __restrict__ res_fg_w, const float* __restrict__ res_fg_b,
-    const float* __restrict__ res_bg_ln_g, const float* __restrict__ res_bg_ln_b,
-    const float* __restrict__ res_bg_w, const float* __restrict__ res_bg_b,
-    const float* __restrict__ q_ln_g, const float* __restrict__ q_ln_b, const float* __restrict__ q_w,
-    const float* __restrict__ qbg_ln_g, const float* __restrict__ qbg_ln_b, const float* __restrict__ qbg_w,
+    const float* __restrict__ gfg_wih, const float* __restrict__ gfg_whh,
+    const float* __restrict__ gfg_bih, const float* __restrict__ gfg_bhh,
+    const float* __restrict__ gbg_wih, const float* __restrict__ gbg_whh,
+    const float* __restrict__ gbg_bih, const float* __restrict__ gbg_bhh,
+    const float* __restrict__ rfg_g, const float* __restrict__ rfg_b2,
+    const float* __restrict__ rfg_w, const float* __restrict__ rfg_bb,
+    const float* __restrict__ rbg_g, const float* __restrict__ rbg_b2,
+    const float* __restrict__ rbg_w, const float* __restrict__ rbg_bb,
     float* __restrict__ dout)
 {
   __shared__ float wl[64];
@@ -573,13 +726,8 @@
     int bk = blk, b = bk >> 2, k = bk & 3;
     if (wv == 0) {
       const float* pp = fgP + ((size_t)(b * NCH + l) * 4 + k) * FG_PS;
-      float mp = pp[0];
-      float sp = pp[1];
-      float pxp = pp[2];
-      float pyp = pp[3];
-      float sxp = pp[4];
-      float syp = pp[5];
-      float smp = pp[6];
+      float mp = pp[0], sp = pp[1], pxp = pp[2], pyp = pp[3];
+      float sxp = pp[4], syp = pp[5], smp = pp[6];
       float mg = rmax_all(mp);
       float w = __expf(mp - mg);
       wl[l] = w;
@@ -605,25 +753,25 @@
       float UV = ubuf[0][l] + ubuf[1][l] + ubuf[2][l] + ubuf[3][l];
       float upd = (UV + scal[3] * cbuf[l] + scal[4] * cbuf[64 + l] - scal[5] * cbuf[128 + l]) / S + cbuf[192 + l];
       xs[l] = upd;
-      hs[l] = slot_fg[bk * 64 + l];
+      hs[l] = slotfg[bk * 64 + l];
     }
     __syncthreads();
     {
       int r = tid;
       float a;
       if (r < 192) {
-        const float* w = gru_fg_wih + r * 64; a = gru_fg_bih[r];
+        const float* w = gfg_wih + r * 64; a = gfg_bih[r];
         #pragma unroll 8
         for (int c = 0; c < 64; ++c) a += w[c] * xs[c];
       } else {
-        const float* w = gru_fg_whh + (r - 192) * 64; a = gru_fg_bhh[r - 192];
+        const float* w = gfg_whh + (r - 192) * 64; a = gfg_bhh[r - 192];
         #pragma unroll 8
         for (int c = 0; c < 64; ++c) a += w[c] * hs[c];
       }
       gd[r] = a;
       if (tid < 128) {
         int r2 = tid + 256;
-        const float* w = gru_fg_whh + (r2 - 192) * 64; float a2 = gru_fg_bhh[r2 - 192];
+        const float* w = gfg_whh + (r2 - 192) * 64; float a2 = gfg_bhh[r2 - 192];
         #pragma unroll 8
         for (int c = 0; c < 64; ++c) a2 += w[c] * hs[c];
         gd[r2] = a2;
@@ -639,12 +787,12 @@
       float mean = rsum_all(hnew) * (1.f / 64.f);
       float d = hnew - mean;
       float var = rsum_all(d * d) * (1.f / 64.f);
-      xs[l] = d * rsqrtf(var + 1e-5f) * res_fg_ln_g[l] + res_fg_ln_b[l];
+      xs[l] = d * rsqrtf(var + 1e-5f) * rfg_g[l] + rfg_b2[l];
     }
     __syncthreads();
     {
       int c0 = wv * 16;
-      const float* w = res_fg_w + l * 64 + c0;
+      const float* w = rfg_w + l * 64 + c0;
       float a = 0;
       #pragma unroll
       for (int c = 0; c < 16; ++c) a += w[c] * xs[c0 + c];
@@ -652,37 +800,11 @@
     }
     __syncthreads();
     if (wv == 0) {
-      float h = hs[l];
-      float snew = part[0][l] + part[1][l] + part[2][l] + part[3][l] + res_fg_b[l] + h;
-      slot_fg[bk * 64 + l] = snew;
+      float snew = part[0][l] + part[1][l] + part[2][l] + part[3][l] + rfg_bb[l] + hs[l];
       dout[(b * 5 + 1 + k) * 64 + l] = snew;
-      float mq = rsum_all(snew) * (1.f / 64.f);
-      float dq = snew - mq;
-      float vq = rsum_all(dq * dq) * (1.f / 64.f);
-      xs[l] = dq * rsqrtf(vq + 1e-5f) * q_ln_g[l] + q_ln_b[l];
-    }
-    __syncthreads();
-    {
-      int c0 = wv * 16;
-      const float* w = q_w + l * 64 + c0;
-      float a = 0;
-      #pragma unroll
-      for (int c = 0; c < 16; ++c) a += w[c] * xs[c0 + c];
-      part[wv][l] = a;
-    }
-    __syncthreads();
-    if (wv == 0) {
-      float qacc = part[0][l] + part[1][l] + part[2][l] + part[3][l];
-      q_fg[bk * 64 + l] = qacc;
-      float qGx = rsum_all(qacc * cbuf[l]);
-      float qGy = rsum_all(qacc * cbuf[64 + l]);
-      float qgW = rsum_all(qacc * cbuf[128 + l]);
-      float qC0 = rsum_all(qacc * cbuf[192 + l]);
       if (l == 0) {
-        qscal[bk*4+0]=qGx; qscal[bk*4+1]=qGy; qscal[bk*4+2]=qgW; qscal[bk*4+3]=qC0;
-        float px = scal[1], py = scal[2];
-        fg_pos[bk * 2 + 0] = px; fg_pos[bk * 2 + 1] = py;
-        dout[1280 + bk * 2 + 0] = px; dout[1280 + bk * 2 + 1] = py;
+        dout[1280 + bk * 2 + 0] = scal[1];
+        dout[1280 + bk * 2 + 1] = scal[2];
       }
     }
   } else {
@@ -712,25 +834,25 @@
       float upd = (ubuf[0][l] + ubuf[1][l] + ubuf[2][l] + ubuf[3][l]) / S
                 + 1e-8f * (part[0][l] + part[1][l] + part[2][l] + part[3][l]);
       xs[l] = upd;
-      hs[l] = slot_bg[b * 64 + l];
+      hs[l] = slotbg[b * 64 + l];
     }
     __syncthreads();
     {
       int r = tid;
       float a;
       if (r < 192) {
-        const float* w = gru_bg_wih + r * 64; a = gru_bg_bih[r];
+        const float* w = gbg_wih + r * 64; a = gbg_bih[r];
         #pragma unroll 8
         for (int c = 0; c < 64; ++c) a += w[c] * xs[c];
       } else {
-        const float* w = gru_bg_whh + (r - 192) * 64; a = gru_bg_bhh[r - 192];
+        const float* w = gbg_whh + (r - 192) * 64; a = gbg_bhh[r - 192];
         #pragma unroll 8
         for (int c = 0; c < 64; ++c) a += w[c] * hs[c];
       }
       gd[r] = a;
       if (tid < 128) {
         int r2 = tid + 256;
-        const float* w = gru_bg_whh + (r2 - 192) * 64; float a2 = gru_bg_bhh[r2 - 192];
+        const float* w = gbg_whh + (r2 - 192) * 64; float a2 = gbg_bhh[r2 - 192];
         #pragma unroll 8
         for (int c = 0; c < 64; ++c) a2 += w[c] * hs[c];
         gd[r2] = a2;
@@ -746,12 +868,12 @@
       float mean = rsum_all(hnew) * (1.f / 64.f);
       float d = hnew - mean;
       float var = rsum_all(d * d) * (1.f / 64.f);
-      xs[l] = d * rsqrtf(var + 1e-5f) * res_bg_ln_g[l] + res_bg_ln_b[l];
+      xs[l] = d * rsqrtf(var + 1e-5f) * rbg_g[l] + rbg_b2[l];
     }
     __syncthreads();
     {
       int c0 = wv * 16;
-      const float* w = res_bg_w + l * 64 + c0;
+      const float* w = rbg_w + l * 64 + c0;
       float a = 0;
       #pragma unroll
       for (int c = 0; c < 16; ++c) a += w[c] * xs[c0 + c];
@@ -759,27 +881,8 @@
     }
     __syncthreads();
     if (wv == 0) {
-      float h = hs[l];
-      float snew = part[0][l] + part[1][l] + part[2][l] + part[3][l] + res_bg_b[l] + h;
-      slot_bg[b * 64 + l] = snew;
+      float snew = part[0][l] + part[1][l] + part[2][l] + part[3][l] + rbg_bb[l] + hs[l];
       dout[(b * 5 + 0) * 64 + l] = snew;
-      float mq = rsum_all(snew) * (1.f / 64.f);
-      float dq = snew - mq;
-      float vq = rsum_all(dq * dq) * (1.f / 64.f);
-      xs[l] = dq * rsqrtf(vq + 1e-5f) * qbg_ln_g[l] + qbg_ln_b[l];
-    }
-    __syncthreads();
-    {
-      int c0 = wv * 16;
-      const float* w = qbg_w + l * 64 + c0;
-      float a = 0;
-      #pragma unroll
-      for (int c = 0; c < 16; ++c) a += w[c] * xs[c0 + c];
-      part[wv][l] = a;
-    }
-    __syncthreads();
-    if (wv == 0) {
-      q_bg[b * 64 + l] = part[0][l] + part[1][l] + part[2][l] + part[3][l];
     }
   }
 }
@@ -849,36 +952,43 @@
   float* statsKV       = (float*)alloc((size_t)Bb * Nn * 8 * 4);
   unsigned short* kbg  = (unsigned short*)alloc((size_t)Bb * Nn * 64 * 2);
   unsigned short* vbg  = (unsigned short*)alloc((size_t)Bb * Nn * 64 * 2);
-  float* slot_fg = (float*)alloc(16 * 64 * 4);
-  float* slot_bg = (float*)alloc(4 * 64 * 4);
+  float* sfg[2]; float* sbg[2]; float* fgP[2]; float* bgP[2];
+  sfg[0] = (float*)alloc(16 * 64 * 4); sfg[1] = (float*)alloc(16 * 64 * 4);
+  sbg[0] = (float*)alloc(4 * 64 * 4);  sbg[1] = (float*)alloc(4 * 64 * 4);
   float* q_fg    = (float*)alloc(16 * 64 * 4);
   float* q_bg    = (float*)alloc(4 * 64 * 4);
   float* fg_pos  = (float*)alloc(16 * 2 * 4);
-  float* qscal   = (float*)alloc(16 * 4 * 4);
   float* cbuf    = (float*)alloc(264 * 4);
-  float* fgP     = (float*)alloc((size_t)Bb * NCH * 4 * FG_PS * 4);
-  float* bgP     = (float*)alloc((size_t)BG_BLK * BG_PS * 4);
-
-  k_setup<<<5, 1024, 0, stream>>>(mask, grid_embed_w, grid_embed_b, mlp_fg_ln_g, mlp_fg_ln_b,
-                                  mlp_fg_w, mlp_fg_b, fg_pos, cbuf);
-  k_prep<<<532, 256, 0, stream>>>(feat, norm_feat_g, norm_feat_b, grid_embed_w, grid_embed_b,
-                                  k_fg_w, v_fg_w, k_bg_w, v_bg_w,
-                                  mlp_bg_ln_g, mlp_bg_ln_b, mlp_bg_w, mlp_bg_b,
-                                  mlp_fg_ln_g, mlp_fg_w,
-                                  A_k, A_vT, statsKV, kbg, vbg,
-                                  noise_fg, noise_bg, slots_mu, slots_ls, slots_mu_bg, slots_ls_bg,
-                                  q_ln_g, q_ln_b, q_w, qbg_ln_g, qbg_ln_b, qbg_w, cbuf,
-                                  slot_fg, slot_bg, q_fg, q_bg, qscal);
+  fgP[0] = (float*)alloc((size_t)Bb * NCH * 4 * FG_PS * 4);
+  fgP[1] = (float*)alloc((size_t)Bb * NCH * 4 * FG_PS * 4);
+  bgP[0] = (float*)alloc((size_t)BG_BLK * BG_PS * 4);
+  bgP[1] = (float*)alloc((size_t)BG_BLK * BG_PS * 4);
+
+  k_prep<<<1049, 256, 0, stream>>>(feat, norm_feat_g, norm_feat_b, grid_embed_w, grid_embed_b,
+                                   k_fg_w, v_fg_w, k_bg_w, v_bg_w,
+                                   mlp_bg_ln_g, mlp_bg_ln_b, mlp_bg_w, mlp_bg_b,
+                                   mlp_fg_ln_g, mlp_fg_ln_b, mlp_fg_w, mlp_fg_b, mask,
+                                   A_k, A_vT, statsKV, kbg, vbg,
+                                   noise_fg, noise_bg, slots_mu, slots_ls, slots_mu_bg, slots_ls_bg,
+                                   q_ln_g, q_ln_b, q_w, qbg_ln_g, qbg_ln_b, qbg_w,
+                                   sfg[0], sbg[0], q_fg, q_bg, fg_pos, cbuf);
   for (int it = 0; it < 4; ++it) {
-    k_iter<<<FG_BLK + BG_BLK, 256, 0, stream>>>(A_k, A_vT, statsKV, kbg, vbg,
-                                                q_fg, q_bg, fg_pos, mask, cbuf, qscal,
-                                                fgP, bgP);
-    k_comb<<<20, 256, 0, stream>>>(fgP, bgP, slot_fg, slot_bg, q_fg, q_bg, fg_pos, qscal, cbuf,
-                                   gru_fg_wih, gru_fg_whh, gru_fg_bih, gru_fg_bhh,
-                                   gru_bg_wih, gru_bg_whh, gru_bg_bih, gru_bg_bhh,
-                                   res_fg_ln_g, res_fg_ln_b, res_fg_w, res_fg_b,
-                                   res_bg_ln_g, res_bg_ln_b, res_bg_w, res_bg_b,
-                                   q_ln_g, q_ln_b, q_w, qbg_ln_g, qbg_ln_b, qbg_w,
-                                   dout);
+    int pr = (it + 1) & 1;
+    int pw = it & 1;
+    k_iter<<<FG_BLK + BG_BLK, 256, 0, stream>>>(it, A_k, A_vT, statsKV, kbg, vbg,
+                                                q_fg, q_bg, fg_pos, mask, cbuf,
+                                                fgP[pr], fgP[pw], bgP[pr], bgP[pw],
+                                                sfg[pr], sfg[pw], sbg[pr], sbg[pw],
+                                                gru_fg_wih, gru_fg_whh, gru_fg_bih, gru_fg_bhh,
+                                                gru_bg_wih, gru_bg_whh, gru_bg_bih, gru_bg_bhh,
+                                                res_fg_ln_g, res_fg_ln_b, res_fg_w, res_fg_b,
+                                                res_bg_ln_g, res_bg_ln_b, res_bg_w, res_bg_b,
+                                                q_ln_g, q_ln_b, q_w, qbg_ln_g, qbg_ln_b, qbg_w);
   }
+  k_fin<<<20, 256, 0, stream>>>(fgP[1], bgP[1], sfg[1], sbg[1], cbuf,
+                                gru_fg_wih, gru_fg_whh, gru_fg_bih, gru_fg_bhh,
+                                gru_bg_wih, gru_bg_whh, gru_bg_bih, gru_bg_bhh,
+                                res_fg_ln_g, res_fg_ln_b, res_fg_w, res_fg_b,
+                                res_bg_ln_g, res_bg_ln_b, res_bg_w, res_bg_b,
+                                dout);
 }
```

After: 160.3 us. 37.2% more time.
